# Optimization experiments

Measured on AMD Instinct MI355X. Metric: run time of the kernel, lower is better.

Reference implementation:

```python
import jax, jax.numpy as jnp
import numpy as np

N, E, F_IN, H, C, Q = 4096, 131072, 512, 64, 16, 6
ALPHA = 1.0
NITER = 2  # torch.svd_lowrank default power iterations


def setup_inputs() -> dict:
    key = jax.random.key(0)
    ks = jax.random.split(key, 12)
    rn = lambda k, s, sc=0.05: jax.random.normal(k, s, dtype=jnp.float32) * sc
    return {
        'x': jax.random.normal(ks[0], (N, F_IN), dtype=jnp.float32),
        'edge_index': jax.random.randint(ks[1], (2, E), 0, N, dtype=jnp.int32),
        'gcn1_w': rn(ks[2], (F_IN, H)), 'gcn1_b': jnp.zeros((H,), jnp.float32),
        'gcn2_w': rn(ks[3], (H, C)), 'gcn2_b': jnp.zeros((C,), jnp.float32),
        'ptd1_w1': rn(ks[4], (F_IN, H)), 'ptd1_b1': jnp.zeros((H,), jnp.float32),
        'ptd1_w2': rn(ks[5], (H, 1)), 'ptd1_b2': jnp.zeros((1,), jnp.float32),
        'ptd2_w1': rn(ks[6], (H, 32)), 'ptd2_b1': jnp.zeros((32,), jnp.float32),
        'ptd2_w2': rn(ks[7], (32, 1)), 'ptd2_b2': jnp.zeros((1,), jnp.float32),
        'omega1': jax.random.normal(ks[8], (N, Q), dtype=jnp.float32),
        'omega2': jax.random.normal(ks[9], (N, Q), dtype=jnp.float32),
    }


def _mlp2(x, w1, b1, w2, b2):
    return jax.nn.relu(x @ w1 + b1) @ w2 + b2


def _edge_gate(x, src, dst, w1, b1, w2, b2):
    # agg = ptd(x_src - x_dst)**2 ; test branch: s = alpha*sigmoid(agg), clipped to [0,1]
    agg = _mlp2(x[src] - x[dst], w1, b1, w2, b2)
    agg = agg * agg
    s = ALPHA * jax.nn.sigmoid(agg)
    return jnp.clip(s.reshape(-1), 0.0, 1.0)


def _gcn_conv(x, src, dst, ew, w, b):
    # PyG GCNConv with edge_weight: add self-loops (weight 1), symmetric norm, aggregate src->dst
    h = x @ w
    si = jnp.arange(N)
    s_full = jnp.concatenate([src, si])
    d_full = jnp.concatenate([dst, si])
    ew_full = jnp.concatenate([ew, jnp.ones((N,), ew.dtype)])
    deg = jax.ops.segment_sum(ew_full, d_full, num_segments=N)
    dis = jnp.where(deg > 0, jax.lax.rsqrt(jnp.maximum(deg, 1e-12)), 0.0)
    norm = dis[s_full] * ew_full * dis[d_full]
    out = jax.ops.segment_sum(norm[:, None] * h[s_full], d_full, num_segments=N)
    return out + b


def _svd_lowrank_V(A, omega):
    # torch.svd_lowrank(A, q=6, niter=2): randomized range finder + small SVD; returns V [N, Q]
    Qb, _ = jnp.linalg.qr(A @ omega)
    for _ in range(NITER):
        Z, _ = jnp.linalg.qr(A.T @ Qb)
        Qb, _ = jnp.linalg.qr(A @ Z)
    B = Qb.T @ A  # [Q, N]
    _, _, Vh = jnp.linalg.svd(B, full_matrices=False)
    return Vh.T  # [N, Q]


def _nuc_loss(aa, V, deflate_matmul):
    loss = jnp.float32(0.0)
    for k in range(Q):  # fixed small Q=6, structurally sequential deflation
        vi = aa @ V[:, k:k + 1]  # [N,1]
        vi = vi / jnp.linalg.norm(vi)
        vmv = (vi.T @ (aa @ vi))[0, 0]
        vv = (vi.T @ vi)[0, 0]
        loss = loss + jnp.sqrt(jnp.abs(vmv / vv))
        if k > 1:
            outer = vi @ vi.T
            aa = aa - (aa @ outer if deflate_matmul else aa * outer)
    return loss


def reference(x, edge_index, gcn1_w, gcn1_b, gcn2_w, gcn2_b,
              ptd1_w1, ptd1_b1, ptd1_w2, ptd1_b2,
              ptd2_w1, ptd2_b1, ptd2_w2, ptd2_b2, omega1, omega2):
    src, dst = edge_index[0], edge_index[1]

    s_1 = _edge_gate(x, src, dst, ptd1_w1, ptd1_b1, ptd1_w2, ptd1_b2)  # [E]
    x1 = jax.nn.relu(_gcn_conv(x, src, dst, s_1, gcn1_w, gcn1_b))  # [N,H], dropout off (eval)

    s_2 = _edge_gate(x1, src, dst, ptd2_w1, ptd2_b1, ptd2_w2, ptd2_b2)  # [E]
    x_out = _gcn_conv(x1, src, dst, s_2, gcn2_w, gcn2_b)  # [N,C]

    # consistency loss: MSE of centered gates against zeros
    consist = jnp.mean((s_1 - jnp.mean(s_1)) ** 2) + jnp.mean((s_2 - jnp.mean(s_2)) ** 2)

    # dense adjacencies (duplicate edges sum, as in to_dense_adj)
    s1d = jnp.zeros((N, N), jnp.float32).at[src, dst].add(s_1) + 1e-6
    s2d = jnp.zeros((N, N), jnp.float32).at[src, dst].add(s_2) + 1e-6
    aa1 = s1d @ s1d.T
    aa2 = s2d @ s2d.T

    V1 = _svd_lowrank_V(s1d, omega1)
    V2 = _svd_lowrank_V(s2d, omega2)
    nuc = _nuc_loss(aa1, V1, deflate_matmul=False) + _nuc_loss(aa2, V2, deflate_matmul=True)

    top2 = jax.lax.top_k(x_out, 2)[0]
    calib = -top2[:, 0] + top2[:, 1]

    return (jax.nn.log_softmax(x_out, axis=1),
            jax.nn.softmax(x_out, axis=1),
            0.01 * consist + 0.01 * nuc,
            s_1, s_2, jnp.mean(calib))
```

## Files before the change

### kernel.cpp

```cpp
#include <hip/hip_runtime.h>
#include <cmath>

constexpr int N = 4096;
constexpr int EDG = 131072;
constexpr float GEPS = 1e-6f;

__device__ __forceinline__ float* blk_sums(float* vals, int cnt) {
  __shared__ float part[4][16];
  __shared__ float tot[16];
  const int lane = threadIdx.x & 63, wv = threadIdx.x >> 6;
  for (int c = 0; c < cnt; ++c) {
    float v = vals[c];
    for (int off = 32; off; off >>= 1) v += __shfl_down(v, off);
    if (lane == 0) part[wv][c] = v;
  }
  __syncthreads();
  if (threadIdx.x == 0)
    for (int c = 0; c < cnt; ++c)
      tot[c] = part[0][c] + part[1][c] + part[2][c] + part[3][c];
  __syncthreads();
  return tot;
}

__global__ void hist_edges(const int* __restrict__ ei, int* __restrict__ cnt) {
  int e = blockIdx.x * 256 + threadIdx.x;
  atomicAdd(&cnt[ei[e]], 1);
  atomicAdd(&cnt[N + ei[EDG + e]], 1);
}

__global__ __launch_bounds__(256) void scan2x(const int* __restrict__ cnt,
                                              int* __restrict__ rowptr,
                                              int* __restrict__ cur) {
  const int b = blockIdx.x;
  const int* c = cnt + b * N;
  int* rp = rowptr + b * (N + 1);
  int* cu = cur + b * N;
  __shared__ int part[256];
  const int t = threadIdx.x;
  int local[16], s = 0;
  const int base = t * 16;
  for (int i = 0; i < 16; ++i) { local[i] = s; s += c[base + i]; }
  part[t] = s;
  __syncthreads();
  if (t == 0) {
    int acc = 0;
    for (int i = 0; i < 256; ++i) { int v = part[i]; part[i] = acc; acc += v; }
  }
  __syncthreads();
  const int off = part[t];
  for (int i = 0; i < 16; ++i) { rp[base + i] = off + local[i]; cu[base + i] = off + local[i]; }
  if (t == 255) rp[N] = off + s;
}

__global__ void scatter_edges(const int* __restrict__ ei, int* __restrict__ cur,
                              int* __restrict__ col_s, int* __restrict__ perm_s,
                              int* __restrict__ col_d, int* __restrict__ perm_d) {
  int e = blockIdx.x * 256 + threadIdx.x;
  int s = ei[e], d = ei[EDG + e];
  int ps = atomicAdd(&cur[s], 1);
  col_s[ps] = d; perm_s[ps] = e;
  int pd = atomicAdd(&cur[N + d], 1);
  col_d[pd] = s; perm_d[pd] = e;
}

__global__ void gather_w2(const float* __restrict__ s, const int* __restrict__ perm_s,
                          const int* __restrict__ perm_d, float* __restrict__ ws_,
                          float* __restrict__ wd_) {
  int p = blockIdx.x * 256 + threadIdx.x;
  ws_[p] = s[perm_s[p]];
  wd_[p] = s[perm_d[p]];
}

template<int F, int DIS>
__global__ __launch_bounds__(256) void spmm(const int* __restrict__ rowptr,
                                            const int* __restrict__ col,
                                            const float* __restrict__ w,
                                            const float* __restrict__ X,
                                            const float* __restrict__ dis,
                                            float* __restrict__ OUT,
                                            float* __restrict__ SC, int cs_idx,
                                            float eps, int osum, int ossq) {
  constexpr int ES = 64 / F;
  const int lane = threadIdx.x & 63;
  const int wv = threadIdx.x >> 6;
  const int f = lane & (F - 1);
  const int es = lane / F;
  const int r = blockIdx.x * 4 + wv;
  const int e0 = rowptr[r], e1 = rowptr[r + 1];
  float acc = 0.f;
  for (int e = e0 + es; e < e1; e += ES) {
    int c = col[e];
    float wx = w[e];
    if (DIS) wx *= dis[c];
    acc += wx * X[(size_t)c * F + f];
  }
#pragma unroll
  for (int off = F; off < 64; off <<= 1) acc += __shfl_xor(acc, off);
  float o = acc + ((cs_idx >= 0) ? eps * SC[cs_idx + f] : 0.f);
  if (es == 0) OUT[(size_t)r * F + f] = o;
  if (osum >= 0 || ossq >= 0) {
    __shared__ float bs[8], bq[8];
    if (threadIdx.x < F) { bs[threadIdx.x] = 0.f; bq[threadIdx.x] = 0.f; }
    __syncthreads();
    if (es == 0) {
      if (osum >= 0) atomicAdd(&bs[f], o);
      if (ossq >= 0) atomicAdd(&bq[f], o * o);
    }
    __syncthreads();
    if (threadIdx.x < F) {
      if (osum >= 0) atomicAdd(&SC[osum + threadIdx.x], bs[threadIdx.x]);
      if (ossq >= 0) atomicAdd(&SC[ossq + threadIdx.x], bq[threadIdx.x]);
    }
  }
}

template<int FA, int FB>
__global__ __launch_bounds__(256) void spmm2(const int* __restrict__ rowptr,
                                             const int* __restrict__ col,
                                             const float* __restrict__ wA,
                                             const float* __restrict__ wB,
                                             const float* __restrict__ XA,
                                             const float* __restrict__ XB,
                                             float* __restrict__ OA,
                                             float* __restrict__ OB,
                                             float* __restrict__ SC,
                                             int csA, int csB, float eps,
                                             int osumA, int ossqA, int osumB, int ossqB) {
  const int lane = threadIdx.x & 63;
  const int wv = threadIdx.x >> 6;
  const int half = lane >> 5;
  const int la = lane & 31;
  const int F = half ? FB : FA;
  const int f = la & (F - 1);
  const int es = la / F;
  const int ES = 32 / F;
  const int r = blockIdx.x * 4 + wv;
  const int e0 = rowptr[r], e1 = rowptr[r + 1];
  const float* w = half ? wB : wA;
  const float* X = half ? XB : XA;
  float acc = 0.f;
  for (int e = e0 + es; e < e1; e += ES)
    acc += w[e] * X[(size_t)col[e] * F + f];
  for (int off = F; off < 32; off <<= 1) acc += __shfl_xor(acc, off);
  const int cs = half ? csB : csA;
  float o = acc + ((cs >= 0) ? eps * SC[cs + f] : 0.f);
  if (es == 0) {
    float* O = half ? OB : OA;
    O[(size_t)r * F + f] = o;
  }
  if (osumA >= 0 || ossqA >= 0 || osumB >= 0 || ossqB >= 0) {
    __shared__ float bs[2][8], bq[2][8];
    if (threadIdx.x < 16) { bs[threadIdx.x >> 3][threadIdx.x & 7] = 0.f;
                            bq[threadIdx.x >> 3][threadIdx.x & 7] = 0.f; }
    __syncthreads();
    const int osum = half ? osumB : osumA, ossq = half ? ossqB : ossqA;
    if (es == 0) {
      if (osum >= 0) atomicAdd(&bs[half][f], o);
      if (ossq >= 0) atomicAdd(&bq[half][f], o * o);
    }
    __syncthreads();
    if (threadIdx.x < 16) {
      int h = threadIdx.x >> 3, ff = threadIdx.x & 7;
      int os_ = h ? osumB : osumA, oq_ = h ? ossqB : ossqA;
      int Fh = h ? FB : FA;
      if (os_ >= 0 && ff < Fh) atomicAdd(&SC[os_ + ff], bs[h][ff]);
      if (oq_ >= 0 && ff < Fh) atomicAdd(&SC[oq_ + ff], bq[h][ff]);
    }
  }
}

__global__ __launch_bounds__(256) void gemm512(const float* __restrict__ A,
                                               const float* __restrict__ W1,
                                               const float* __restrict__ W2,
                                               float* __restrict__ O1,
                                               float* __restrict__ O2) {
  __shared__ float As[16][33];
  __shared__ float Ws[32][128];
  const int t = threadIdx.x;
  const int r = t >> 4;
  const int cg = t & 15;
  const int r0 = blockIdx.x * 16;
  float acc[8];
#pragma unroll
  for (int j = 0; j < 8; ++j) acc[j] = 0.f;
  for (int k0 = 0; k0 < 512; k0 += 32) {
    __syncthreads();
    {
      int idx = t;
#pragma unroll
      for (int i = 0; i < 2; ++i, idx += 256) {
        int rr = idx >> 5, kk = idx & 31;
        As[rr][kk] = A[(size_t)(r0 + rr) * 512 + k0 + kk];
      }
    }
    for (int idx = t; idx < 32 * 128; idx += 256) {
      int kk = idx >> 7, c = idx & 127;
      Ws[kk][c] = (c < 64) ? W1[(size_t)(k0 + kk) * 64 + c]
                           : W2[(size_t)(k0 + kk) * 64 + c - 64];
    }
    __syncthreads();
#pragma unroll 4
    for (int kk = 0; kk < 32; ++kk) {
      float a = As[r][kk];
      const float* wr = &Ws[kk][cg * 8];
#pragma unroll
      for (int j = 0; j < 8; ++j) acc[j] += a * wr[j];
    }
  }
  int n = r0 + r;
  if (cg < 8) {
#pragma unroll
    for (int j = 0; j < 8; ++j) O1[(size_t)n * 64 + cg * 8 + j] = acc[j];
  } else {
#pragma unroll
    for (int j = 0; j < 8; ++j) O2[(size_t)n * 64 + (cg - 8) * 8 + j] = acc[j];
  }
}

__global__ __launch_bounds__(256) void gemm64(const float* __restrict__ A,
                                              const float* __restrict__ W1,
                                              const float* __restrict__ W2,
                                              float* __restrict__ O1,
                                              float* __restrict__ O2) {
  __shared__ float As[32][65];
  __shared__ float Ws[64][48];
  const int t = threadIdx.x;
  const int r = t >> 3;
  const int cg = t & 7;
  const int r0 = blockIdx.x * 32;
  for (int idx = t; idx < 32 * 64; idx += 256)
    As[idx >> 6][idx & 63] = A[(size_t)(r0 + (idx >> 6)) * 64 + (idx & 63)];
  for (int idx = t; idx < 64 * 48; idx += 256) {
    int kk = idx / 48, c = idx % 48;
    Ws[kk][c] = (c < 32) ? W1[kk * 32 + c] : W2[kk * 16 + c - 32];
  }
  __syncthreads();
  float acc[6] = {0.f, 0.f, 0.f, 0.f, 0.f, 0.f};
  for (int k = 0; k < 64; ++k) {
    float a = As[r][k];
#pragma unroll
    for (int j = 0; j < 6; ++j) acc[j] += a * Ws[k][cg + 8 * j];
  }
  int n = r0 + r;
#pragma unroll
  for (int j = 0; j < 6; ++j) {
    int c = cg + 8 * j;
    if (c < 32) O1[(size_t)n * 32 + c] = acc[j];
    else O2[(size_t)n * 16 + c - 32] = acc[j];
  }
}

__global__ void edge_gate1(const float* __restrict__ xw, const int* __restrict__ ei,
                           const float* __restrict__ b1, const float* __restrict__ w2,
                           const float* __restrict__ b2, float* __restrict__ s_out,
                           float* __restrict__ deg, float* __restrict__ SCs) {
  const int lane = threadIdx.x & 63;
  const int wave = threadIdx.x >> 6;
  const float b1v = b1[lane];
  const float w2v = w2[lane];
  const float b2s = b2[0];
  float lsum = 0.f, lssq = 0.f;
  for (int it = 0; it < 16; ++it) {
    const int e = blockIdx.x * 64 + it * 4 + wave;
    const int s = ei[e];
    const int d = ei[EDG + e];
    float g = xw[(size_t)s * 64 + lane] - xw[(size_t)d * 64 + lane] + b1v;
    g = fmaxf(g, 0.f) * w2v;
#pragma unroll
    for (int off = 32; off; off >>= 1) g += __shfl_down(g, off);
    if (lane == 0) {
      float agg = g + b2s;
      agg *= agg;
      float sv = 1.f / (1.f + __expf(-agg));
      s_out[e] = sv;
      atomicAdd(&deg[d], sv);
      lsum += sv; lssq += sv * sv;
    }
  }
  __shared__ float red[8];
  if (lane == 0) { red[wave] = lsum; red[4 + wave] = lssq; }
  __syncthreads();
  if (threadIdx.x == 0) {
    atomicAdd(&SCs[0], red[0] + red[1] + red[2] + red[3]);
    atomicAdd(&SCs[1], red[4] + red[5] + red[6] + red[7]);
  }
}

__global__ void edge_gate2(const float* __restrict__ xw, const int* __restrict__ ei,
                           const float* __restrict__ b1, const float* __restrict__ w2,
                           const float* __restrict__ b2, float* __restrict__ s_out,
                           float* __restrict__ deg, float* __restrict__ SCs) {
  const int half = threadIdx.x & 31;
  const int wi = threadIdx.x >> 5;
  const float b1v = b1[half];
  const float w2v = w2[half];
  const float b2s = b2[0];
  float lsum = 0.f, lssq = 0.f;
  for (int it = 0; it < 16; ++it) {
    const int e = blockIdx.x * 128 + it * 8 + wi;
    const int s = ei[e];
    const int d = ei[EDG + e];
    float g = xw[(size_t)s * 32 + half] - xw[(size_t)d * 32 + half] + b1v;
    g = fmaxf(g, 0.f) * w2v;
#pragma unroll
    for (int off = 16; off; off >>= 1) g += __shfl_down(g, off, 32);
    if (half == 0) {
      float agg = g + b2s;
      agg *= agg;
      float sv = 1.f / (1.f + __expf(-agg));
      s_out[e] = sv;
      atomicAdd(&deg[d], sv);
      lsum += sv; lssq += sv * sv;
    }
  }
  __shared__ float red[16];
  if (half == 0) { red[wi] = lsum; red[8 + wi] = lssq; }
  __syncthreads();
  if (threadIdx.x == 0) {
    float a = 0.f, b = 0.f;
    for (int i = 0; i < 8; ++i) { a += red[i]; b += red[8 + i]; }
    atomicAdd(&SCs[0], a);
    atomicAdd(&SCs[1], b);
  }
}

__global__ void make_dis(const float* __restrict__ deg, float* __restrict__ dis) {
  int n = blockIdx.x * 256 + threadIdx.x;
  dis[n] = rsqrtf(deg[n] + 1.0f);
}

__global__ void conv_epi64(const float* __restrict__ P, const float* __restrict__ h,
                           const float* __restrict__ dis, const float* __restrict__ bias,
                           float* __restrict__ out) {
  int i = blockIdx.x * 256 + threadIdx.x;
  int n = i >> 6, f = i & 63;
  float d = dis[n];
  float v = d * (P[i] + d * h[i]) + bias[f];
  out[i] = fmaxf(v, 0.f);
}

__global__ void conv2_softmax(const float* __restrict__ P, const float* __restrict__ h,
                              const float* __restrict__ dis, const float* __restrict__ bias,
                              float* __restrict__ ls, float* __restrict__ sm,
                              float* __restrict__ SC) {
  const int t = threadIdx.x;
  const int r = blockIdx.x * 256 + t;
  const float d = dis[r];
  float v[16];
  float mx = -3.0e38f, mx2 = -3.0e38f;
#pragma unroll
  for (int c = 0; c < 16; ++c) {
    v[c] = d * (P[(size_t)r * 16 + c] + d * h[(size_t)r * 16 + c]) + bias[c];
    if (v[c] > mx) { mx2 = mx; mx = v[c]; }
    else if (v[c] > mx2) mx2 = v[c];
  }
  float se = 0.f;
#pragma unroll
  for (int c = 0; c < 16; ++c) se += expf(v[c] - mx);
  const float lse = mx + logf(se);
#pragma unroll
  for (int c = 0; c < 16; ++c) {
    float z = v[c] - lse;
    ls[(size_t)r * 16 + c] = z;
    sm[(size_t)r * 16 + c] = expf(z);
  }
  float calib = mx2 - mx;
  float* tot = blk_sums(&calib, 1);
  if (t == 0) atomicAdd(&SC[4], tot[0]);
}

__global__ void gram2(const float* __restrict__ YA, const float* __restrict__ YB,
                      double* __restrict__ GA, double* __restrict__ GB) {
  const int t = threadIdx.x;
  const int lane = t & 63, wv = t >> 6;
  const int n = blockIdx.x * 256 + t;
  float g[42];
  {
    float ya[6], yb[6];
#pragma unroll
    for (int j = 0; j < 6; ++j) { ya[j] = YA[(size_t)n * 8 + j]; yb[j] = YB[(size_t)n * 8 + j]; }
    int p = 0;
#pragma unroll
    for (int i = 0; i < 6; ++i)
#pragma unroll
      for (int j = i; j < 6; ++j) { g[p] = ya[i] * ya[j]; g[21 + p] = yb[i] * yb[j]; ++p; }
  }
#pragma unroll
  for (int p = 0; p < 42; ++p)
    for (int off = 32; off; off >>= 1) g[p] += __shfl_down(g[p], off);
  __shared__ float part[4][42];
  if (lane == 0)
    for (int p = 0; p < 42; ++p) part[wv][p] = g[p];
  __syncthreads();
  if (t < 42) {
    float s = part[0][t] + part[1][t] + part[2][t] + part[3][t];
    if (t < 21) atomicAdd(&GA[t], (double)s);
    else atomicAdd(&GB[t - 21], (double)s);
  }
}

__global__ void chol2(float* __restrict__ YA, const double* __restrict__ GA, int csA,
                      float* __restrict__ YB, const double* __restrict__ GB, int csB,
                      float* __restrict__ SC) {
  __shared__ float Rs[2][36];
  if (threadIdx.x < 2) {
    const double* G = threadIdx.x ? GB : GA;
    double Gf[6][6];
    int p = 0;
    for (int i = 0; i < 6; ++i)
      for (int j = i; j < 6; ++j) { Gf[i][j] = G[p]; Gf[j][i] = G[p]; ++p; }
    double Rm[6][6];
    for (int i = 0; i < 6; ++i) for (int j = 0; j < 6; ++j) Rm[i][j] = 0.0;
    for (int j = 0; j < 6; ++j) {
      double s = Gf[j][j];
      for (int k = 0; k < j; ++k) s -= Rm[k][j] * Rm[k][j];
      double dj = sqrt(fmax(s, 1e-30));
      Rm[j][j] = dj;
      for (int i = j + 1; i < 6; ++i) {
        double v = Gf[j][i];
        for (int k = 0; k < j; ++k) v -= Rm[k][j] * Rm[k][i];
        Rm[j][i] = v / dj;
      }
    }
    for (int i = 0; i < 6; ++i)
      for (int j = 0; j < 6; ++j) Rs[threadIdx.x][i * 6 + j] = (float)Rm[i][j];
  }
  __syncthreads();
  int n = blockIdx.x * 256 + threadIdx.x;
  float vals[12];
  {
    float y[6], q[6];
#pragma unroll
    for (int j = 0; j < 6; ++j) y[j] = YA[(size_t)n * 8 + j];
#pragma unroll
    for (int j = 0; j < 6; ++j) {
      float s = y[j];
#pragma unroll
      for (int i = 0; i < 6; ++i)
        if (i < j) s -= q[i] * Rs[0][i * 6 + j];
      q[j] = s / Rs[0][j * 6 + j];
    }
#pragma unroll
    for (int j = 0; j < 6; ++j) { YA[(size_t)n * 8 + j] = q[j]; vals[j] = q[j]; }
  }
  {
    float y[6], q[6];
#pragma unroll
    for (int j = 0; j < 6; ++j) y[j] = YB[(size_t)n * 8 + j];
#pragma unroll
    for (int j = 0; j < 6; ++j) {
      float s = y[j];
#pragma unroll
      for (int i = 0; i < 6; ++i)
        if (i < j) s -= q[i] * Rs[1][i * 6 + j];
      q[j] = s / Rs[1][j * 6 + j];
    }
#pragma unroll
    for (int j = 0; j < 6; ++j) { YB[(size_t)n * 8 + j] = q[j]; vals[6 + j] = q[j]; }
  }
  float* tot = blk_sums(vals, 12);
  if (threadIdx.x == 0)
    for (int j = 0; j < 6; ++j) {
      atomicAdd(&SC[csA + j], tot[j]);
      atomicAdd(&SC[csB + j], tot[6 + j]);
    }
}

__global__ __launch_bounds__(128) void jacobi2(const double* __restrict__ GA,
                                               const double* __restrict__ GB,
                                               float* __restrict__ SMFA,
                                               float* __restrict__ SMFB) {
  const int wv = threadIdx.x >> 6;
  const int lane = threadIdx.x & 63;
  const double* G = wv ? GB : GA;
  float* SMF = wv ? SMFB : SMFA;
  double a[6], v[6];
#pragma unroll
  for (int j = 0; j < 6; ++j) { a[j] = 0.0; v[j] = 0.0; }
  if (lane < 6) {
    const int r = lane;
    for (int j = 0; j < 6; ++j) {
      int i0 = r < j ? r : j, j0 = r < j ? j : r;
      a[j] = G[i0 * 6 - i0 * (i0 - 1) / 2 + (j0 - i0)];
    }
    v[r] = 1.0;
  }
  for (int sweep = 0; sweep < 10; ++sweep) {
#pragma unroll
    for (int p = 0; p < 5; ++p)
#pragma unroll
      for (int q = p + 1; q < 6; ++q) {
        double apq = __shfl(a[q], p, 64);
        double app = __shfl(a[p], p, 64);
        double aqq = __shfl(a[q], q, 64);
        double c = 1.0, s = 0.0;
        if (fabs(apq) > 1e-300) {
          double tau = (aqq - app) / (2.0 * apq);
          double tt = (tau >= 0.0) ? 1.0 / (tau + sqrt(1.0 + tau * tau))
                                   : 1.0 / (tau - sqrt(1.0 + tau * tau));
          c = 1.0 / sqrt(1.0 + tt * tt); s = tt * c;
        }
        double ap_ = a[p], aq_ = a[q];
        a[p] = c * ap_ - s * aq_;
        a[q] = s * ap_ + c * aq_;
#pragma unroll
        for (int i = 0; i < 6; ++i) {
          double rp = __shfl(a[i], p, 64);
          double rq = __shfl(a[i], q, 64);
          if (lane == p) a[i] = c * rp - s * rq;
          if (lane == q) a[i] = s * rp + c * rq;
        }
        double vp_ = v[p], vq_ = v[q];
        v[p] = c * vp_ - s * vq_;
        v[q] = s * vp_ + c * vq_;
      }
  }
  __shared__ double diag[2][6];
  __shared__ double Vs[2][6][6];
  if (lane < 6) {
    diag[wv][lane] = a[lane];
    for (int j = 0; j < 6; ++j) Vs[wv][lane][j] = v[j];
  }
  __syncthreads();
  if (lane == 0) {
    int idx[6] = {0, 1, 2, 3, 4, 5};
    for (int x = 0; x < 5; ++x)
      for (int b = 0; b < 5 - x; ++b)
        if (diag[wv][idx[b]] < diag[wv][idx[b + 1]]) {
          int tmp = idx[b]; idx[b] = idx[b + 1]; idx[b + 1] = tmp;
        }
    for (int k = 0; k < 6; ++k) {
      double lam = diag[wv][idx[k]];
      SMF[36 + k] = (float)(1.0 / sqrt(fmax(lam, 1e-30)));
      for (int j = 0; j < 6; ++j) SMF[j * 6 + k] = (float)Vs[wv][j][idx[k]];
    }
  }
}

__global__ void v_scale2(const float* __restrict__ BtA, const float* __restrict__ SMFA,
                         const float* __restrict__ BtB, const float* __restrict__ SMFB,
                         float* __restrict__ V8A, float* __restrict__ V8B) {
  __shared__ float WsA[36], rsA[6], WsB[36], rsB[6];
  if (threadIdx.x < 36) { WsA[threadIdx.x] = SMFA[threadIdx.x]; WsB[threadIdx.x] = SMFB[threadIdx.x]; }
  if (threadIdx.x < 6) { rsA[threadIdx.x] = SMFA[36 + threadIdx.x]; rsB[threadIdx.x] = SMFB[36 + threadIdx.x]; }
  __syncthreads();
  int n = blockIdx.x * 256 + threadIdx.x;
  float ba[6], bb[6];
#pragma unroll
  for (int j = 0; j < 6; ++j) { ba[j] = BtA[(size_t)n * 8 + j]; bb[j] = BtB[(size_t)n * 8 + j]; }
#pragma unroll
  for (int k = 0; k < 6; ++k) {
    float sa = 0.f, sb = 0.f;
#pragma unroll
    for (int j = 0; j < 6; ++j) { sa += ba[j] * WsA[j * 6 + k]; sb += bb[j] * WsB[j * 6 + k]; }
    V8A[(size_t)n * 8 + k] = sa * rsA[k];
    V8B[(size_t)n * 8 + k] = sb * rsB[k];
  }
  V8A[(size_t)n * 8 + 6] = 0.f; V8A[(size_t)n * 8 + 7] = 0.f;
  V8B[(size_t)n * 8 + 6] = 0.f; V8B[(size_t)n * 8 + 7] = 0.f;
}

__global__ void pad8c2(const float* __restrict__ o1, float* __restrict__ d1,
                       const float* __restrict__ o2, float* __restrict__ d2,
                       float* __restrict__ SC, int s1, int s2) {
  int n = blockIdx.x * 256 + threadIdx.x;
  float vals[12];
#pragma unroll
  for (int k = 0; k < 6; ++k) {
    vals[k] = o1[(size_t)n * 6 + k];     d1[(size_t)n * 8 + k] = vals[k];
    vals[6 + k] = o2[(size_t)n * 6 + k]; d2[(size_t)n * 8 + k] = vals[6 + k];
  }
  d1[(size_t)n * 8 + 6] = 0.f; d1[(size_t)n * 8 + 7] = 0.f;
  d2[(size_t)n * 8 + 6] = 0.f; d2[(size_t)n * 8 + 7] = 0.f;
  float* tot = blk_sums(vals, 12);
  if (threadIdx.x == 0)
    for (int c = 0; c < 6; ++c) {
      atomicAdd(&SC[s1 + c], tot[c]);
      atomicAdd(&SC[s2 + c], tot[6 + c]);
    }
}

__global__ void pack3c2(const float* __restrict__ V8A, float* __restrict__ WA,
                        const float* __restrict__ V8B, float* __restrict__ WB,
                        float* __restrict__ SC, int sA, int sB) {
  int n = blockIdx.x * 256 + threadIdx.x;
  float vals[6];
#pragma unroll
  for (int k = 0; k < 3; ++k) {
    vals[k] = V8A[(size_t)n * 8 + k];     WA[(size_t)n * 4 + k] = vals[k];
    vals[3 + k] = V8B[(size_t)n * 8 + k]; WB[(size_t)n * 4 + k] = vals[3 + k];
  }
  WA[(size_t)n * 4 + 3] = 0.f;
  WB[(size_t)n * 4 + 3] = 0.f;
  float* tot = blk_sums(vals, 6);
  if (threadIdx.x == 0)
    for (int c = 0; c < 3; ++c) {
      atomicAdd(&SC[sA + c], tot[c]);
      atomicAdd(&SC[sB + c], tot[3 + c]);
    }
}

__global__ void build_Wc(float* __restrict__ out, int FCpad, int nterms, int nu,
                         const float* __restrict__ base, int bstride, int boff,
                         const float* __restrict__ U, const float* __restrict__ SCin,
                         int rs_idx, float* __restrict__ SC, int sum_idx) {
  int n = blockIdx.x * 256 + threadIdx.x;
  float bv = base[(size_t)n * bstride + boff];
  if (rs_idx >= 0) bv *= rsqrtf(SCin[rs_idx]);
  float uv[3];
  for (int b = 0; b < 3; ++b) uv[b] = (b < nu) ? U[(size_t)b * N + n] : 0.f;
  float vals[8];
  for (int t = 0; t < FCpad; ++t) {
    float v = 0.f;
    if (t < nterms) {
      v = bv;
      for (int b = 0; b < nu; ++b)
        if ((t >> b) & 1) v *= uv[b];
    }
    out[(size_t)n * FCpad + t] = v;
    vals[t] = v;
  }
  float* tot = blk_sums(vals, nterms);
  if (threadIdx.x == 0)
    for (int c = 0; c < nterms; ++c) atomicAdd(&SC[sum_idx + c], tot[c]);
}

__global__ void buildAB(float* __restrict__ WA, int FCpad, int nt, int nu,
                        const float* __restrict__ V8A, int kcol,
                        const float* __restrict__ UvA, float* __restrict__ SC, int sWa,
                        float* __restrict__ WB, const float* __restrict__ V8B,
                        const float* __restrict__ UvB, int nd, int sWb, int Cidx) {
  const int bid = blockIdx.x;
  const int n = (bid & 15) * 256 + threadIdx.x;
  if (bid < 16) {
    float bv = V8A[(size_t)n * 8 + kcol];
    float uv[3];
    for (int b = 0; b < 3; ++b) uv[b] = (b < nu) ? UvA[(size_t)b * N + n] : 0.f;
    float vals[8];
    for (int t = 0; t < FCpad; ++t) {
      float v = 0.f;
      if (t < nt) {
        v = bv;
        for (int b = 0; b < nu; ++b)
          if ((t >> b) & 1) v *= uv[b];
      }
      WA[(size_t)n * FCpad + t] = v;
      vals[t] = v;
    }
    float* tot = blk_sums(vals, nt);
    if (threadIdx.x == 0)
      for (int c = 0; c < nt; ++c) atomicAdd(&SC[sWa + c], tot[c]);
  } else {
    float v = V8B[(size_t)n * 8 + kcol];
    WB[(size_t)n * 4 + 0] = v;
    WB[(size_t)n * 4 + 1] = 0.f;
    WB[(size_t)n * 4 + 2] = 0.f;
    WB[(size_t)n * 4 + 3] = 0.f;
    float vals[4];
    vals[0] = v;
    for (int t = 0; t < 3; ++t) vals[1 + t] = (t < nd) ? UvB[(size_t)t * N + n] * v : 0.f;
    float* tot = blk_sums(vals, 1 + nd);
    if (threadIdx.x == 0) {
      atomicAdd(&SC[sWb], tot[0]);
      for (int t = 0; t < nd; ++t) atomicAdd(&SC[Cidx + t], tot[1 + t]);
    }
  }
}

__global__ void epiAB(const float* __restrict__ YA, int FA, int nt, int nu,
                      const float* __restrict__ UvA, float* __restrict__ yvA, int nyA2,
                      const float* __restrict__ YB, const float* __restrict__ Pv,
                      const float* __restrict__ UvB, int nd, float* __restrict__ yvB,
                      int Cidx, int nyB2, int dp, float* __restrict__ SC) {
  const int bid = blockIdx.x;
  const int n = (bid & 15) * 256 + threadIdx.x;
  if (bid < 16) {
    float uv[3];
    for (int b = 0; b < 3; ++b) uv[b] = (b < nu) ? UvA[(size_t)b * N + n] : 0.f;
    float s = 0.f;
    for (int t = 0; t < nt; ++t) {
      float w = YA[(size_t)n * FA + t];
      int pc = 0;
      for (int b = 0; b < nu; ++b)
        if ((t >> b) & 1) { w *= uv[b]; ++pc; }
      s += (pc & 1) ? -w : w;
    }
    yvA[n] = s;
    float v = s * s;
    float* tot = blk_sums(&v, 1);
    if (threadIdx.x == 0) atomicAdd(&SC[nyA2], tot[0]);
  } else {
    float y = YB[(size_t)n * 4];
    for (int t = 0; t < nd; ++t) y -= SC[Cidx + t] * Pv[(size_t)t * N + n];
    yvB[n] = y;
    float vals[7];
    vals[0] = y * y;
    for (int t = 0; t < 3; ++t) {
      vals[1 + 2 * t] = (t < nd) ? y * Pv[(size_t)t * N + n] : 0.f;
      vals[2 + 2 * t] = (t < nd) ? UvB[(size_t)t * N + n] * y : 0.f;
    }
    float* tot = blk_sums(vals, 1 + 2 * nd);
    if (threadIdx.x == 0) {
      atomicAdd(&SC[nyB2], tot[0]);
      for (int i = 0; i < 2 * nd; ++i) atomicAdd(&SC[dp + i], tot[1 + i]);
    }
  }
}

__global__ void buildAB2(float* __restrict__ WA, int FCpad, int nt, int nu,
                         const float* __restrict__ yvA, const float* __restrict__ UvA,
                         int sW2a, float* __restrict__ WB,
                         const float* __restrict__ yvB, int sW2b,
                         float* __restrict__ SC) {
  const int bid = blockIdx.x;
  const int n = (bid & 15) * 256 + threadIdx.x;
  if (bid < 16) {
    float bv = yvA[n];
    float uv[3];
    for (int b = 0; b < 3; ++b) uv[b] = (b < nu) ? UvA[(size_t)b * N + n] : 0.f;
    float vals[8];
    for (int t = 0; t < FCpad; ++t) {
      float v = 0.f;
      if (t < nt) {
        v = bv;
        for (int b = 0; b < nu; ++b)
          if ((t >> b) & 1) v *= uv[b];
      }
      WA[(size_t)n * FCpad + t] = v;
      vals[t] = v;
    }
    float* tot = blk_sums(vals, nt);
    if (threadIdx.x == 0)
      for (int c = 0; c < nt; ++c) atomicAdd(&SC[sW2a + c], tot[c]);
  } else {
    float v = yvB[n];
    WB[(size_t)n * 4 + 0] = v;
    WB[(size_t)n * 4 + 1] = 0.f;
    WB[(size_t)n * 4 + 2] = 0.f;
    WB[(size_t)n * 4 + 3] = 0.f;
    float vv = v;
    float* tot = blk_sums(&vv, 1);
    if (threadIdx.x == 0) atomicAdd(&SC[sW2b], tot[0]);
  }
}

__global__ void vscale2(float* __restrict__ o1, const float* __restrict__ i1,
                        int s1, int f1, int r1,
                        float* __restrict__ o2, const float* __restrict__ i2,
                        int s2, int f2, int r2, const float* __restrict__ SC) {
  int n = blockIdx.x * 256 + threadIdx.x;
  float v1 = i1[(size_t)n * s1 + f1];
  if (r1 >= 0) v1 *= rsqrtf(SC[r1]);
  o1[n] = v1;
  float v2 = i2[(size_t)n * s2 + f2];
  if (r2 >= 0) v2 *= rsqrtf(SC[r2]);
  o2[n] = v2;
}

__global__ void vscale1(float* __restrict__ out, const float* __restrict__ in,
                        int stride, int off, const float* __restrict__ SC, int rs_idx) {
  int n = blockIdx.x * 256 + threadIdx.x;
  float v = in[(size_t)n * stride + off];
  if (rs_idx >= 0) v *= rsqrtf(SC[rs_idx]);
  out[n] = v;
}

__global__ void axpy_sq(float* __restrict__ out, const float* __restrict__ Y, int stride,
                        int off, const float* __restrict__ q0, const float* __restrict__ q1,
                        const float* __restrict__ q2, float* __restrict__ SC,
                        int c0, int c1, int c2, int np, int coef_rs, int out_rs,
                        int ssq_idx) {
  int n = blockIdx.x * 256 + threadIdx.x;
  float crs = (coef_rs >= 0) ? rsqrtf(SC[coef_rs]) : 1.f;
  float s = Y[(size_t)n * stride + off];
  if (np > 0) s -= SC[c0] * crs * q0[n];
  if (np > 1) s -= SC[c1] * crs * q1[n];
  if (np > 2) s -= SC[c2] * crs * q2[n];
  if (out_rs >= 0) s *= rsqrtf(SC[out_rs]);
  out[n] = s;
  if (ssq_idx >= 0) {
    float v = s * s;
    float* tot = blk_sums(&v, 1);
    if (threadIdx.x == 0) atomicAdd(&SC[ssq_idx], tot[0]);
  }
}

__global__ void accum2b(float* __restrict__ SC, int zA, int nyA, int zB, int nyB) {
  if (threadIdx.x || blockIdx.x) return;
  float add = 0.f;
  for (int k = 0; k < 3; ++k) add += sqrtf(fabsf(SC[zA + k] / SC[nyA + k]));
  for (int k = 0; k < 3; ++k) add += sqrtf(fabsf(SC[zB + k] / SC[nyB + k]));
  SC[5] += add;
}

__global__ void accum2k(float* __restrict__ SC, int zzA, int nt, int nyA,
                        int zzB, int nyB, int dp, int nd) {
  if (threadIdx.x || blockIdx.x) return;
  float vmv = 0.f;
  for (int t = 0; t < nt; ++t) {
    int pc = __popc(t);
    vmv += (pc & 1) ? -SC[zzA + t] : SC[zzA + t];
  }
  float add = sqrtf(fabsf(vmv / SC[nyA]));
  float vb = SC[zzB];
  for (int t = 0; t < nd; ++t) vb -= SC[dp + 2 * t] * SC[dp + 2 * t + 1];
  add += sqrtf(fabsf(vb / SC[nyB]));
  SC[5] += add;
}

__global__ void finalize_k(const float* __restrict__ SC, float* __restrict__ out) {
  if (threadIdx.x || blockIdx.x) return;
  const float Ef = (float)EDG;
  float m1 = SC[0] / Ef, v1 = SC[1] / Ef - m1 * m1;
  float m2 = SC[2] / Ef, v2 = SC[3] / Ef - m2 * m2;
  out[131072] = 0.01f * (v1 + v2) + 0.01f * SC[5];
  out[393217] = SC[4] / (float)N;
}

extern "C" void kernel_launch(void* const* d_in, const int* in_sizes, int n_in,
                              void* d_out, int out_size, void* d_ws, size_t ws_size,
                              hipStream_t stream) {
  const float* x      = (const float*)d_in[0];
  const int*   ei     = (const int*)  d_in[1];
  const float* gcn1_w = (const float*)d_in[2];
  const float* gcn1_b = (const float*)d_in[3];
  const float* gcn2_w = (const float*)d_in[4];
  const float* gcn2_b = (const float*)d_in[5];
  const float* p1w1   = (const float*)d_in[6];
  const float* p1b1   = (const float*)d_in[7];
  const float* p1w2   = (const float*)d_in[8];
  const float* p1b2   = (const float*)d_in[9];
  const float* p2w1   = (const float*)d_in[10];
  const float* p2b1   = (const float*)d_in[11];
  const float* p2w2   = (const float*)d_in[12];
  const float* p2b2   = (const float*)d_in[13];
  const float* omega1 = (const float*)d_in[14];
  const float* omega2 = (const float*)d_in[15];
  float* out = (float*)d_out;

  float* ws = (float*)d_ws;
  size_t o = 0;
  auto alloc = [&](size_t nf) { float* p = ws + o; o += nf; return p; };
  float* xw1  = alloc((size_t)N * 64);
  float* h1   = alloc((size_t)N * 64);
  float* x1   = alloc((size_t)N * 64);
  float* P    = alloc((size_t)N * 64);
  float* x1w  = alloc((size_t)N * 32);
  float* h2   = alloc((size_t)N * 16);
  float* P2   = alloc((size_t)N * 16);
  float* dis1 = alloc(N);
  float* dis2 = alloc(N);
  float* OmA  = alloc((size_t)N * 8);
  float* OmB  = alloc((size_t)N * 8);
  float* QA   = alloc((size_t)N * 8);
  float* QB   = alloc((size_t)N * 8);
  float* ZA   = alloc((size_t)N * 8);
  float* ZB   = alloc((size_t)N * 8);
  float* BtA  = alloc((size_t)N * 8);
  float* BtB  = alloc((size_t)N * 8);
  float* V8A  = alloc((size_t)N * 8);
  float* V8B  = alloc((size_t)N * 8);
  float* WA   = alloc((size_t)N * 8);
  float* WB   = alloc((size_t)N * 4);
  float* TA   = alloc((size_t)N * 8);
  float* TB   = alloc((size_t)N * 4);
  float* YA   = alloc((size_t)N * 8);
  float* YB   = alloc((size_t)N * 4);
  float* ZZA  = alloc((size_t)N * 8);
  float* ZZB  = alloc((size_t)N * 4);
  float* P4   = alloc((size_t)N * 4);
  float* yvA  = alloc(N);
  float* yvB  = alloc(N);
  float* UvA  = alloc((size_t)3 * N);
  float* UvB  = alloc((size_t)3 * N);
  float* Pv   = alloc((size_t)3 * N);
  float* SMFA = alloc(64);
  float* SMFB = alloc(64);
  int* rowptr = (int*)alloc(2 * (N + 1) + 2);
  int* cur    = (int*)alloc(2 * N);
  int* col_s  = (int*)alloc(EDG);
  int* perm_s = (int*)alloc(EDG);
  int* col_d  = (int*)alloc(EDG);
  int* perm_d = (int*)alloc(EDG);
  float* w1s  = alloc(EDG);
  float* w1d  = alloc(EDG);
  float* w2s  = alloc(EDG);
  float* w2d  = alloc(EDG);
  o = (o + 1) & ~(size_t)1;
  float* zb = ws + o;
  double* Gd = (double*)zb;            o += 288 * 2;
  int* cnt   = (int*)(ws + o);         o += 2 * N;
  float* deg1 = alloc(N);
  float* deg2 = alloc(N);
  float* SC   = alloc(1024);
  const size_t zero_bytes = (576 + 2 * N + 2 * N + 1024) * sizeof(float);
  if (ws_size < o * sizeof(float)) return;

  const int* rp_s = rowptr;
  const int* rp_d = rowptr + (N + 1);

  int cs = 8;
  auto NS = [&]() { int s = cs; cs += 8; return s; };
  int gslot = 0;
  auto NG = [&]() { int g = gslot; gslot += 24; return g; };

  hipMemsetAsync(zb, 0, zero_bytes, stream);
  hist_edges<<<512, 256, 0, stream>>>(ei, cnt);
  scan2x<<<2, 256, 0, stream>>>(cnt, rowptr, cur);
  scatter_edges<<<512, 256, 0, stream>>>(ei, cur, col_s, perm_s, col_d, perm_d);

  gemm512<<<256, 256, 0, stream>>>(x, p1w1, gcn1_w, xw1, h1);
  edge_gate1<<<2048, 256, 0, stream>>>(xw1, ei, p1b1, p1w2, p1b2,
                                       out + 131073, deg1, SC + 0);
  gather_w2<<<512, 256, 0, stream>>>(out + 131073, perm_s, perm_d, w1s, w1d);
  make_dis<<<16, 256, 0, stream>>>(deg1, dis1);
  spmm<64, 1><<<1024, 256, 0, stream>>>(rp_d, col_d, w1d, h1, dis1, P, SC, -1, 0.f, -1, -1);
  conv_epi64<<<1024, 256, 0, stream>>>(P, h1, dis1, gcn1_b, x1);

  gemm64<<<128, 256, 0, stream>>>(x1, p2w1, gcn2_w, x1w, h2);
  edge_gate2<<<1024, 256, 0, stream>>>(x1w, ei, p2b1, p2w2, p2b2,
                                       out + 262145, deg2, SC + 2);
  gather_w2<<<512, 256, 0, stream>>>(out + 262145, perm_s, perm_d, w2s, w2d);
  make_dis<<<16, 256, 0, stream>>>(deg2, dis2);
  spmm<16, 1><<<1024, 256, 0, stream>>>(rp_d, col_d, w2d, h2, dis2, P2, SC, -1, 0.f, -1, -1);
  conv2_softmax<<<16, 256, 0, stream>>>(P2, h2, dis2, gcn2_b, out, out + 65536, SC);

  {
    int s0a = NS(), s0b = NS();
    pad8c2<<<16, 256, 0, stream>>>(omega1, OmA, omega2, OmB, SC, s0a, s0b);
    spmm2<8, 8><<<1024, 256, 0, stream>>>(rp_s, col_s, w1s, w2s, OmA, OmB, QA, QB,
                                          SC, s0a, s0b, GEPS, -1, -1, -1, -1);
    int g0a = NG(), g0b = NG();
    gram2<<<16, 256, 0, stream>>>(QA, QB, Gd + g0a, Gd + g0b);
    int cqa = NS(), cqb = NS();
    chol2<<<16, 256, 0, stream>>>(QA, Gd + g0a, cqa, QB, Gd + g0b, cqb, SC);
    for (int itp = 0; itp < 2; ++itp) {
      spmm2<8, 8><<<1024, 256, 0, stream>>>(rp_d, col_d, w1d, w2d, QA, QB, ZA, ZB,
                                            SC, cqa, cqb, GEPS, -1, -1, -1, -1);
      int gza = NG(), gzb = NG();
      gram2<<<16, 256, 0, stream>>>(ZA, ZB, Gd + gza, Gd + gzb);
      int cza = NS(), czb = NS();
      chol2<<<16, 256, 0, stream>>>(ZA, Gd + gza, cza, ZB, Gd + gzb, czb, SC);
      spmm2<8, 8><<<1024, 256, 0, stream>>>(rp_s, col_s, w1s, w2s, ZA, ZB, QA, QB,
                                            SC, cza, czb, GEPS, -1, -1, -1, -1);
      int gqa = NG(), gqb = NG();
      gram2<<<16, 256, 0, stream>>>(QA, QB, Gd + gqa, Gd + gqb);
      cqa = NS(); cqb = NS();
      chol2<<<16, 256, 0, stream>>>(QA, Gd + gqa, cqa, QB, Gd + gqb, cqb, SC);
    }
    spmm2<8, 8><<<1024, 256, 0, stream>>>(rp_d, col_d, w1d, w2d, QA, QB, BtA, BtB,
                                          SC, cqa, cqb, GEPS, -1, -1, -1, -1);
    int gba = NG(), gbb = NG();
    gram2<<<16, 256, 0, stream>>>(BtA, BtB, Gd + gba, Gd + gbb);
    jacobi2<<<1, 128, 0, stream>>>(Gd + gba, Gd + gbb, SMFA, SMFB);
    v_scale2<<<16, 256, 0, stream>>>(BtA, SMFA, BtB, SMFB, V8A, V8B);
  }

  int nyB0;
  {
    int sWa = NS(), sWb = NS();
    pack3c2<<<16, 256, 0, stream>>>(V8A, WA, V8B, WB, SC, sWa, sWb);
    int sTa = NS(), sTb = NS();
    spmm2<4, 4><<<1024, 256, 0, stream>>>(rp_d, col_d, w1d, w2d, WA, WB, TA, TB,
                                          SC, sWa, sWb, GEPS, sTa, -1, sTb, -1);
    int sYa = NS(), sYb = NS(), nyA = NS(), nyB = NS();
    spmm2<4, 4><<<1024, 256, 0, stream>>>(rp_s, col_s, w1s, w2s, TA, TB, YA, YB,
                                          SC, sTa, sTb, GEPS, sYa, nyA, sYb, nyB);
    int zzA = NS(), zzB = NS();
    spmm2<4, 4><<<1024, 256, 0, stream>>>(rp_d, col_d, w1d, w2d, YA, YB, ZZA, ZZB,
                                          SC, sYa, sYb, GEPS, -1, zzA, -1, zzB);
    accum2b<<<1, 1, 0, stream>>>(SC, zzA, nyA, zzB, nyB);
    vscale2<<<16, 256, 0, stream>>>(UvA, YA, 4, 2, nyA + 2,
                                    UvB, YB, 4, 2, nyB + 2, SC);
    nyB0 = nyB;
  }

  {
    int sWp = NS();
    build_Wc<<<16, 256, 0, stream>>>(WB, 4, 1, 0, ZZB, 4, 2, nullptr, SC, nyB0 + 2, SC, sWp);
    spmm<4, 0><<<1024, 256, 0, stream>>>(rp_s, col_s, w2s, WB, nullptr, P4, SC, sWp, GEPS, -1, -1);
    vscale1<<<16, 256, 0, stream>>>(Pv, P4, 4, 0, SC, -1);
  }

  for (int k = 3; k <= 5; ++k) {
    const int nu = k - 2, nt = 1 << nu, nd = k - 2;
    const int FA = (k < 5) ? 4 : 8;
    int sWa = NS(), sWb = NS(), C = NS(), sTa = NS(), sTb = NS();
    int nyA2 = NS(), nyB2 = NS(), sW2a = NS(), sW2b = NS(), zzA2 = NS(), zzB2 = NS(), dp = NS();
    buildAB<<<32, 256, 0, stream>>>(WA, FA, nt, nu, V8A, k, UvA, SC, sWa,
                                    WB, V8B, UvB, nd, sWb, C);
    if (FA == 4) {
      spmm2<4, 4><<<1024, 256, 0, stream>>>(rp_d, col_d, w1d, w2d, WA, WB, TA, TB,
                                            SC, sWa, sWb, GEPS, sTa, -1, sTb, -1);
      spmm2<4, 4><<<1024, 256, 0, stream>>>(rp_s, col_s, w1s, w2s, TA, TB, YA, YB,
                                            SC, sTa, sTb, GEPS, -1, -1, -1, -1);
    } else {
      spmm2<8, 4><<<1024, 256, 0, stream>>>(rp_d, col_d, w1d, w2d, WA, WB, TA, TB,
                                            SC, sWa, sWb, GEPS, sTa, -1, sTb, -1);
      spmm2<8, 4><<<1024, 256, 0, stream>>>(rp_s, col_s, w1s, w2s, TA, TB, YA, YB,
                                            SC, sTa, sTb, GEPS, -1, -1, -1, -1);
    }
    epiAB<<<32, 256, 0, stream>>>(YA, FA, nt, nu, UvA, yvA, nyA2,
                                  YB, Pv, UvB, nd, yvB, C, nyB2, dp, SC);
    buildAB2<<<32, 256, 0, stream>>>(WA, FA, nt, nu, yvA, UvA, sW2a,
                                     WB, yvB, sW2b, SC);
    if (FA == 4)
      spmm2<4, 4><<<1024, 256, 0, stream>>>(rp_d, col_d, w1d, w2d, WA, WB, ZZA, ZZB,
                                            SC, sW2a, sW2b, GEPS, -1, zzA2, -1, zzB2);
    else
      spmm2<8, 4><<<1024, 256, 0, stream>>>(rp_d, col_d, w1d, w2d, WA, WB, ZZA, ZZB,
                                            SC, sW2a, sW2b, GEPS, -1, zzA2, -1, zzB2);
    accum2k<<<1, 1, 0, stream>>>(SC, zzA2, nt, nyA2, zzB2, nyB2, dp, nd);
    if (k < 5) {
      vscale2<<<16, 256, 0, stream>>>(UvA + (size_t)(k - 2) * N, yvA, 1, 0, nyA2,
                                      UvB + (size_t)(k - 2) * N, yvB, 1, 0, nyB2, SC);
      int sW3 = NS();
      build_Wc<<<16, 256, 0, stream>>>(WB, 4, 1, 0, ZZB, 4, 0, nullptr, SC, nyB2, SC, sW3);
      spmm<4, 0><<<1024, 256, 0, stream>>>(rp_s, col_s, w2s, WB, nullptr, P4, SC, sW3, GEPS, -1, -1);
      axpy_sq<<<16, 256, 0, stream>>>(Pv + (size_t)(k - 2) * N, P4, 4, 0,
                                      Pv, Pv + N, Pv + 2 * N,
                                      SC, dp + 1, dp + 3, dp + 5, nd, nyB2, -1, -1);
    }
  }

  finalize_k<<<1, 1, 0, stream>>>(SC, out);
}
```

Baseline: 863.4 us.

## Restructure pipeline with fused conv, softmax, Cholesky-QR power iteration kernels

Replaces large parts of the host-side launch sequence and many kernels. The gather kernel now also computes degree rsqrt and omega column sums. GCN convolutions get dedicated fused kernels with self-loop and bias folded in, and softmax/log-softmax/top-2 calibration share one kernel. The randomized SVD range finder now uses an spmm kernel that applies an in-kernel Cholesky-QR normalization from the accumulated Gram matrix, and the 512-wide GEMM is split along K with atomic accumulation. Several small post-processing launches in the deflation loop are merged. The aim is fewer launches and fewer passes over memory, at the cost of atomics, double-precision Gram accumulation, and more complex numerics that could differ from the reference.

```diff
diff --git a/kernel.cpp b/kernel.cpp
--- a/kernel.cpp
+++ b/kernel.cpp
@@ -63,12 +63,375 @@
   col_d[pd] = s; perm_d[pd] = e;
 }
 
-__global__ void gather_w2(const float* __restrict__ s, const int* __restrict__ perm_s,
-                          const int* __restrict__ perm_d, float* __restrict__ ws_,
-                          float* __restrict__ wd_) {
+__global__ void gatherdis_om(const float* __restrict__ s, const int* __restrict__ perm_s,
+                             const int* __restrict__ perm_d, float* __restrict__ ws_,
+                             float* __restrict__ wd_, const float* __restrict__ deg,
+                             float* __restrict__ dis, const float* __restrict__ om1,
+                             const float* __restrict__ om2, float* __restrict__ SC,
+                             int omA, int omB) {
   int p = blockIdx.x * 256 + threadIdx.x;
   ws_[p] = s[perm_s[p]];
   wd_[p] = s[perm_d[p]];
+  if (p < N) dis[p] = rsqrtf(deg[p] + 1.0f);
+  if (om1 && blockIdx.x < 16) {
+    int n = p;
+    float vals[12];
+#pragma unroll
+    for (int k = 0; k < 6; ++k) {
+      vals[k] = om1[(size_t)n * 6 + k];
+      vals[6 + k] = om2[(size_t)n * 6 + k];
+    }
+    float* tot = blk_sums(vals, 12);
+    if (threadIdx.x == 0)
+      for (int c = 0; c < 6; ++c) {
+        atomicAdd(&SC[omA + c], tot[c]);
+        atomicAdd(&SC[omB + c], tot[6 + c]);
+      }
+  }
+}
+
+__global__ __launch_bounds__(256) void gemm512k(const float* __restrict__ A,
+                                                const float* __restrict__ W1,
+                                                const float* __restrict__ W2,
+                                                float* __restrict__ O1,
+                                                float* __restrict__ O2) {
+  __shared__ float As[16][33];
+  __shared__ float Ws[32][128];
+  const int t = threadIdx.x;
+  const int rt = t >> 4;
+  const int ct = t & 15;
+  const int r0 = blockIdx.x * 16;
+  const int kh = blockIdx.y * 256;
+  float acc[8];
+#pragma unroll
+  for (int j = 0; j < 8; ++j) acc[j] = 0.f;
+  for (int kc = 0; kc < 256; kc += 32) {
+    const int kb = kh + kc;
+    __syncthreads();
+    for (int i = t; i < 512; i += 256) {
+      int rr = i >> 5, kk = i & 31;
+      As[rr][kk] = A[(size_t)(r0 + rr) * 512 + kb + kk];
+    }
+    for (int i = t; i < 1024; i += 256) {
+      int row = i >> 5, c4 = i & 31;
+      float4 v;
+      if (c4 < 16) v = *(const float4*)&W1[(size_t)(kb + row) * 64 + c4 * 4];
+      else         v = *(const float4*)&W2[(size_t)(kb + row) * 64 + (c4 - 16) * 4];
+      *(float4*)&Ws[row][c4 * 4] = v;
+    }
+    __syncthreads();
+#pragma unroll
+    for (int kk = 0; kk < 32; ++kk) {
+      float a = As[rt][kk];
+      float4 b0 = *(const float4*)&Ws[kk][ct * 4];
+      float4 b1 = *(const float4*)&Ws[kk][64 + ct * 4];
+      acc[0] += a * b0.x; acc[1] += a * b0.y;
+      acc[2] += a * b0.z; acc[3] += a * b0.w;
+      acc[4] += a * b1.x; acc[5] += a * b1.y;
+      acc[6] += a * b1.z; acc[7] += a * b1.w;
+    }
+  }
+  const int r = r0 + rt;
+#pragma unroll
+  for (int j = 0; j < 4; ++j) {
+    atomicAdd(&O1[(size_t)r * 64 + ct * 4 + j], acc[j]);
+    atomicAdd(&O2[(size_t)r * 64 + ct * 4 + j], acc[4 + j]);
+  }
+}
+
+__global__ __launch_bounds__(256) void gemm64(const float* __restrict__ A,
+                                              const float* __restrict__ W1,
+                                              const float* __restrict__ W2,
+                                              float* __restrict__ O1,
+                                              float* __restrict__ O2) {
+  __shared__ float As[32][65];
+  __shared__ float Ws[64][48];
+  const int t = threadIdx.x;
+  const int r = t >> 3;
+  const int cg = t & 7;
+  const int r0 = blockIdx.x * 32;
+  for (int idx = t; idx < 32 * 64; idx += 256)
+    As[idx >> 6][idx & 63] = A[(size_t)(r0 + (idx >> 6)) * 64 + (idx & 63)];
+  for (int idx = t; idx < 64 * 48; idx += 256) {
+    int kk = idx / 48, c = idx % 48;
+    Ws[kk][c] = (c < 32) ? W1[kk * 32 + c] : W2[kk * 16 + c - 32];
+  }
+  __syncthreads();
+  float acc[6] = {0.f, 0.f, 0.f, 0.f, 0.f, 0.f};
+  for (int k = 0; k < 64; ++k) {
+    float a = As[r][k];
+#pragma unroll
+    for (int j = 0; j < 6; ++j) acc[j] += a * Ws[k][cg + 8 * j];
+  }
+  int n = r0 + r;
+#pragma unroll
+  for (int j = 0; j < 6; ++j) {
+    int c = cg + 8 * j;
+    if (c < 32) O1[(size_t)n * 32 + c] = acc[j];
+    else O2[(size_t)n * 16 + c - 32] = acc[j];
+  }
+}
+
+__global__ void edge_gate1(const float* __restrict__ xw, const int* __restrict__ ei,
+                           const float* __restrict__ b1, const float* __restrict__ w2,
+                           const float* __restrict__ b2, float* __restrict__ s_out,
+                           float* __restrict__ deg, float* __restrict__ SCs) {
+  const int lane = threadIdx.x & 63;
+  const int wave = threadIdx.x >> 6;
+  const float b1v = b1[lane];
+  const float w2v = w2[lane];
+  const float b2s = b2[0];
+  float lsum = 0.f, lssq = 0.f;
+  for (int it = 0; it < 16; ++it) {
+    const int e = blockIdx.x * 64 + it * 4 + wave;
+    const int s = ei[e];
+    const int d = ei[EDG + e];
+    float g = xw[(size_t)s * 64 + lane] - xw[(size_t)d * 64 + lane] + b1v;
+    g = fmaxf(g, 0.f) * w2v;
+#pragma unroll
+    for (int off = 32; off; off >>= 1) g += __shfl_down(g, off);
+    if (lane == 0) {
+      float agg = g + b2s;
+      agg *= agg;
+      float sv = 1.f / (1.f + __expf(-agg));
+      s_out[e] = sv;
+      atomicAdd(&deg[d], sv);
+      lsum += sv; lssq += sv * sv;
+    }
+  }
+  __shared__ float red[8];
+  if (lane == 0) { red[wave] = lsum; red[4 + wave] = lssq; }
+  __syncthreads();
+  if (threadIdx.x == 0) {
+    atomicAdd(&SCs[0], red[0] + red[1] + red[2] + red[3]);
+    atomicAdd(&SCs[1], red[4] + red[5] + red[6] + red[7]);
+  }
+}
+
+__global__ void edge_gate2(const float* __restrict__ xw, const int* __restrict__ ei,
+                           const float* __restrict__ b1, const float* __restrict__ w2,
+                           const float* __restrict__ b2, float* __restrict__ s_out,
+                           float* __restrict__ deg, float* __restrict__ SCs) {
+  const int half = threadIdx.x & 31;
+  const int wi = threadIdx.x >> 5;
+  const float b1v = b1[half];
+  const float w2v = w2[half];
+  const float b2s = b2[0];
+  float lsum = 0.f, lssq = 0.f;
+  for (int it = 0; it < 16; ++it) {
+    const int e = blockIdx.x * 128 + it * 8 + wi;
+    const int s = ei[e];
+    const int d = ei[EDG + e];
+    float g = xw[(size_t)s * 32 + half] - xw[(size_t)d * 32 + half] + b1v;
+    g = fmaxf(g, 0.f) * w2v;
+#pragma unroll
+    for (int off = 16; off; off >>= 1) g += __shfl_down(g, off, 32);
+    if (half == 0) {
+      float agg = g + b2s;
+      agg *= agg;
+      float sv = 1.f / (1.f + __expf(-agg));
+      s_out[e] = sv;
+      atomicAdd(&deg[d], sv);
+      lsum += sv; lssq += sv * sv;
+    }
+  }
+  __shared__ float red[16];
+  if (half == 0) { red[wi] = lsum; red[8 + wi] = lssq; }
+  __syncthreads();
+  if (threadIdx.x == 0) {
+    float a = 0.f, b = 0.f;
+    for (int i = 0; i < 8; ++i) { a += red[i]; b += red[8 + i]; }
+    atomicAdd(&SCs[0], a);
+    atomicAdd(&SCs[1], b);
+  }
+}
+
+__global__ void conv1f(const int* __restrict__ rp, const int* __restrict__ cl,
+                       const float* __restrict__ w, const float* __restrict__ h1,
+                       const float* __restrict__ dis, const float* __restrict__ bias,
+                       float* __restrict__ x1) {
+  const int lane = threadIdx.x & 63, wv = threadIdx.x >> 6;
+  const int r = blockIdx.x * 4 + wv;
+  const int e0 = rp[r], e1 = rp[r + 1];
+  float acc = 0.f;
+  for (int e = e0; e < e1; ++e) {
+    int c = cl[e];
+    acc += w[e] * dis[c] * h1[(size_t)c * 64 + lane];
+  }
+  float d = dis[r];
+  float v = d * (acc + d * h1[(size_t)r * 64 + lane]) + bias[lane];
+  x1[(size_t)r * 64 + lane] = fmaxf(v, 0.f);
+}
+
+__global__ void conv2f(const int* __restrict__ rp, const int* __restrict__ cl,
+                       const float* __restrict__ w, const float* __restrict__ h2,
+                       const float* __restrict__ dis, const float* __restrict__ bias,
+                       float* __restrict__ xo) {
+  const int lane = threadIdx.x & 63, wv = threadIdx.x >> 6;
+  const int f = lane & 15, es = lane >> 4;
+  const int r = blockIdx.x * 4 + wv;
+  const int e0 = rp[r], e1 = rp[r + 1];
+  float acc = 0.f;
+  for (int e = e0 + es; e < e1; e += 4) {
+    int c = cl[e];
+    acc += w[e] * dis[c] * h2[(size_t)c * 16 + f];
+  }
+  acc += __shfl_xor(acc, 16);
+  acc += __shfl_xor(acc, 32);
+  if (es == 0) {
+    float d = dis[r];
+    xo[(size_t)r * 16 + f] = d * (acc + d * h2[(size_t)r * 16 + f]) + bias[f];
+  }
+}
+
+__global__ void softmax_calib(const float* __restrict__ xo, float* __restrict__ ls,
+                              float* __restrict__ sm, float* __restrict__ SC) {
+  const int t = threadIdx.x;
+  const int r = blockIdx.x * 256 + t;
+  float v[16];
+  float mx = -3.0e38f, mx2 = -3.0e38f;
+#pragma unroll
+  for (int c = 0; c < 16; ++c) {
+    v[c] = xo[(size_t)r * 16 + c];
+    if (v[c] > mx) { mx2 = mx; mx = v[c]; }
+    else if (v[c] > mx2) mx2 = v[c];
+  }
+  float se = 0.f;
+#pragma unroll
+  for (int c = 0; c < 16; ++c) se += expf(v[c] - mx);
+  const float lse = mx + logf(se);
+#pragma unroll
+  for (int c = 0; c < 16; ++c) {
+    float z = v[c] - lse;
+    ls[(size_t)r * 16 + c] = z;
+    sm[(size_t)r * 16 + c] = expf(z);
+  }
+  float calib = mx2 - mx;
+  float* tot = blk_sums(&calib, 1);
+  if (t == 0) atomicAdd(&SC[4], tot[0]);
+}
+
+template<int NORM, int SX>
+__global__ __launch_bounds__(256) void spmm8f(
+    const int* __restrict__ rp, const int* __restrict__ cl,
+    const float* __restrict__ wA, const float* __restrict__ wB,
+    const float* __restrict__ XA, const float* __restrict__ XB,
+    float* __restrict__ OA, float* __restrict__ OB,
+    const double* __restrict__ GpA, const double* __restrict__ GpB,
+    double* __restrict__ GnA, double* __restrict__ GnB,
+    float* __restrict__ SC, int cspA, int cspB, int csoA, int csoB) {
+  __shared__ float Rinv[2][36];
+  __shared__ float csn[2][8];
+  __shared__ float bs[2][8];
+  __shared__ float gpart[8][21];
+  const int t = threadIdx.x;
+  if (NORM) {
+    if (t < 2) {
+      const double* G = t ? GpB : GpA;
+      const float* csp = SC + (t ? cspB : cspA);
+      double Gf[6][6];
+      int p = 0;
+      for (int i = 0; i < 6; ++i)
+        for (int j = i; j < 6; ++j) { Gf[i][j] = G[p]; Gf[j][i] = G[p]; ++p; }
+      double Rm[6][6];
+      for (int i = 0; i < 6; ++i) for (int j = 0; j < 6; ++j) Rm[i][j] = 0.0;
+      for (int j = 0; j < 6; ++j) {
+        double s = Gf[j][j];
+        for (int k = 0; k < j; ++k) s -= Rm[k][j] * Rm[k][j];
+        double dj = sqrt(fmax(s, 1e-30));
+        Rm[j][j] = dj;
+        for (int i = j + 1; i < 6; ++i) {
+          double v = Gf[j][i];
+          for (int k = 0; k < j; ++k) v -= Rm[k][j] * Rm[k][i];
+          Rm[j][i] = v / dj;
+        }
+      }
+      double Ri[6][6];
+      for (int j = 0; j < 6; ++j) {
+        Ri[j][j] = 1.0 / Rm[j][j];
+        for (int i = j - 1; i >= 0; --i) {
+          double s = 0.0;
+          for (int k = i + 1; k <= j; ++k) s += Rm[i][k] * Ri[k][j];
+          Ri[i][j] = -s / Rm[i][i];
+        }
+      }
+      for (int i = 0; i < 6; ++i)
+        for (int j = 0; j < 6; ++j)
+          Rinv[t][i * 6 + j] = (j >= i) ? (float)Ri[i][j] : 0.f;
+      for (int f = 0; f < 8; ++f) {
+        float s = 0.f;
+        if (f < 6)
+          for (int j = 0; j <= f; ++j) s += csp[j] * (float)Ri[j][f];
+        csn[t][f] = s;
+      }
+    }
+  } else {
+    if (t < 16) {
+      int h = t >> 3, f = t & 7;
+      csn[h][f] = (f < 6) ? SC[(h ? cspB : cspA) + f] : 0.f;
+    }
+  }
+  if (t < 16) bs[t >> 3][t & 7] = 0.f;
+  __syncthreads();
+  const int lane = t & 63, wv = t >> 6;
+  const int half = lane >> 5, la = lane & 31;
+  const int f = la & 7, es = la >> 3;
+  const float* w = half ? wB : wA;
+  const float* X = half ? XB : XA;
+  float* O = half ? OB : OA;
+  const float* Ri = Rinv[half];
+  const float epsf = csn[half][f] * GEPS;
+  float gp[6];
+#pragma unroll
+  for (int j = 0; j < 6; ++j) gp[j] = 0.f;
+  for (int rr = 0; rr < 2; ++rr) {
+    const int r = blockIdx.x * 8 + wv * 2 + rr;
+    const int e0 = rp[r], e1 = rp[r + 1];
+    float acc = 0.f;
+    if (f < 6) {
+      for (int e = e0 + es; e < e1; e += 4) {
+        int c = cl[e];
+        const float* xr = X + (size_t)c * SX;
+        float xn;
+        if (NORM) {
+          xn = 0.f;
+          for (int j = 0; j <= f; ++j) xn += xr[j] * Ri[j * 6 + f];
+        } else {
+          xn = xr[f];
+        }
+        acc += w[e] * xn;
+      }
+    }
+    acc += __shfl_xor(acc, 8);
+    acc += __shfl_xor(acc, 16);
+    float o = acc + epsf;
+    float ov[6];
+#pragma unroll
+    for (int j = 0; j < 6; ++j) ov[j] = __shfl(o, half * 32 + j);
+    if (es == 0) {
+      O[((size_t)r << 3) + f] = o;
+      if (f < 6) {
+        atomicAdd(&bs[half][f], o);
+#pragma unroll
+        for (int j = 0; j < 6; ++j)
+          if (j >= f) gp[j - f] += o * ov[j];
+      }
+    }
+  }
+  if (es == 0 && f < 6) {
+    int p0 = f * 6 - (f * (f - 1)) / 2;
+    for (int j = 0; j < 6 - f; ++j) gpart[wv * 2 + half][p0 + j] = gp[j];
+  }
+  __syncthreads();
+  if (t < 42) {
+    int h = t / 21, p = t % 21;
+    float s = gpart[h][p] + gpart[2 + h][p] + gpart[4 + h][p] + gpart[6 + h][p];
+    atomicAdd(&(h ? GnB : GnA)[p], (double)s);
+  }
+  if (t < 16) {
+    int h = t >> 3, ff = t & 7;
+    if (ff < 6) atomicAdd(&SC[(h ? csoB : csoA) + ff], bs[h][ff]);
+  }
 }
 
 template<int F, int DIS>
@@ -169,303 +532,6 @@
   }
 }
 
-__global__ __launch_bounds__(256) void gemm512(const float* __restrict__ A,
-                                               const float* __restrict__ W1,
-                                               const float* __restrict__ W2,
-                                               float* __restrict__ O1,
-                                               float* __restrict__ O2) {
-  __shared__ float As[16][33];
-  __shared__ float Ws[32][128];
-  const int t = threadIdx.x;
-  const int r = t >> 4;
-  const int cg = t & 15;
-  const int r0 = blockIdx.x * 16;
-  float acc[8];
-#pragma unroll
-  for (int j = 0; j < 8; ++j) acc[j] = 0.f;
-  for (int k0 = 0; k0 < 512; k0 += 32) {
-    __syncthreads();
-    {
-      int idx = t;
-#pragma unroll
-      for (int i = 0; i < 2; ++i, idx += 256) {
-        int rr = idx >> 5, kk = idx & 31;
-        As[rr][kk] = A[(size_t)(r0 + rr) * 512 + k0 + kk];
-      }
-    }
-    for (int idx = t; idx < 32 * 128; idx += 256) {
-      int kk = idx >> 7, c = idx & 127;
-      Ws[kk][c] = (c < 64) ? W1[(size_t)(k0 + kk) * 64 + c]
-                           : W2[(size_t)(k0 + kk) * 64 + c - 64];
-    }
-    __syncthreads();
-#pragma unroll 4
-    for (int kk = 0; kk < 32; ++kk) {
-      float a = As[r][kk];
-      const float* wr = &Ws[kk][cg * 8];
-#pragma unroll
-      for (int j = 0; j < 8; ++j) acc[j] += a * wr[j];
-    }
-  }
-  int n = r0 + r;
-  if (cg < 8) {
-#pragma unroll
-    for (int j = 0; j < 8; ++j) O1[(size_t)n * 64 + cg * 8 + j] = acc[j];
-  } else {
-#pragma unroll
-    for (int j = 0; j < 8; ++j) O2[(size_t)n * 64 + (cg - 8) * 8 + j] = acc[j];
-  }
-}
-
-__global__ __launch_bounds__(256) void gemm64(const float* __restrict__ A,
-                                              const float* __restrict__ W1,
-                                              const float* __restrict__ W2,
-                                              float* __restrict__ O1,
-                                              float* __restrict__ O2) {
-  __shared__ float As[32][65];
-  __shared__ float Ws[64][48];
-  const int t = threadIdx.x;
-  const int r = t >> 3;
-  const int cg = t & 7;
-  const int r0 = blockIdx.x * 32;
-  for (int idx = t; idx < 32 * 64; idx += 256)
-    As[idx >> 6][idx & 63] = A[(size_t)(r0 + (idx >> 6)) * 64 + (idx & 63)];
-  for (int idx = t; idx < 64 * 48; idx += 256) {
-    int kk = idx / 48, c = idx % 48;
-    Ws[kk][c] = (c < 32) ? W1[kk * 32 + c] : W2[kk * 16 + c - 32];
-  }
-  __syncthreads();
-  float acc[6] = {0.f, 0.f, 0.f, 0.f, 0.f, 0.f};
-  for (int k = 0; k < 64; ++k) {
-    float a = As[r][k];
-#pragma unroll
-    for (int j = 0; j < 6; ++j) acc[j] += a * Ws[k][cg + 8 * j];
-  }
-  int n = r0 + r;
-#pragma unroll
-  for (int j = 0; j < 6; ++j) {
-    int c = cg + 8 * j;
-    if (c < 32) O1[(size_t)n * 32 + c] = acc[j];
-    else O2[(size_t)n * 16 + c - 32] = acc[j];
-  }
-}
-
-__global__ void edge_gate1(const float* __restrict__ xw, const int* __restrict__ ei,
-                           const float* __restrict__ b1, const float* __restrict__ w2,
-                           const float* __restrict__ b2, float* __restrict__ s_out,
-                           float* __restrict__ deg, float* __restrict__ SCs) {
-  const int lane = threadIdx.x & 63;
-  const int wave = threadIdx.x >> 6;
-  const float b1v = b1[lane];
-  const float w2v = w2[lane];
-  const float b2s = b2[0];
-  float lsum = 0.f, lssq = 0.f;
-  for (int it = 0; it < 16; ++it) {
-    const int e = blockIdx.x * 64 + it * 4 + wave;
-    const int s = ei[e];
-    const int d = ei[EDG + e];
-    float g = xw[(size_t)s * 64 + lane] - xw[(size_t)d * 64 + lane] + b1v;
-    g = fmaxf(g, 0.f) * w2v;
-#pragma unroll
-    for (int off = 32; off; off >>= 1) g += __shfl_down(g, off);
-    if (lane == 0) {
-      float agg = g + b2s;
-      agg *= agg;
-      float sv = 1.f / (1.f + __expf(-agg));
-      s_out[e] = sv;
-      atomicAdd(&deg[d], sv);
-      lsum += sv; lssq += sv * sv;
-    }
-  }
-  __shared__ float red[8];
-  if (lane == 0) { red[wave] = lsum; red[4 + wave] = lssq; }
-  __syncthreads();
-  if (threadIdx.x == 0) {
-    atomicAdd(&SCs[0], red[0] + red[1] + red[2] + red[3]);
-    atomicAdd(&SCs[1], red[4] + red[5] + red[6] + red[7]);
-  }
-}
-
-__global__ void edge_gate2(const float* __restrict__ xw, const int* __restrict__ ei,
-                           const float* __restrict__ b1, const float* __restrict__ w2,
-                           const float* __restrict__ b2, float* __restrict__ s_out,
-                           float* __restrict__ deg, float* __restrict__ SCs) {
-  const int half = threadIdx.x & 31;
-  const int wi = threadIdx.x >> 5;
-  const float b1v = b1[half];
-  const float w2v = w2[half];
-  const float b2s = b2[0];
-  float lsum = 0.f, lssq = 0.f;
-  for (int it = 0; it < 16; ++it) {
-    const int e = blockIdx.x * 128 + it * 8 + wi;
-    const int s = ei[e];
-    const int d = ei[EDG + e];
-    float g = xw[(size_t)s * 32 + half] - xw[(size_t)d * 32 + half] + b1v;
-    g = fmaxf(g, 0.f) * w2v;
-#pragma unroll
-    for (int off = 16; off; off >>= 1) g += __shfl_down(g, off, 32);
-    if (half == 0) {
-      float agg = g + b2s;
-      agg *= agg;
-      float sv = 1.f / (1.f + __expf(-agg));
-      s_out[e] = sv;
-      atomicAdd(&deg[d], sv);
-      lsum += sv; lssq += sv * sv;
-    }
-  }
-  __shared__ float red[16];
-  if (half == 0) { red[wi] = lsum; red[8 + wi] = lssq; }
-  __syncthreads();
-  if (threadIdx.x == 0) {
-    float a = 0.f, b = 0.f;
-    for (int i = 0; i < 8; ++i) { a += red[i]; b += red[8 + i]; }
-    atomicAdd(&SCs[0], a);
-    atomicAdd(&SCs[1], b);
-  }
-}
-
-__global__ void make_dis(const float* __restrict__ deg, float* __restrict__ dis) {
-  int n = blockIdx.x * 256 + threadIdx.x;
-  dis[n] = rsqrtf(deg[n] + 1.0f);
-}
-
-__global__ void conv_epi64(const float* __restrict__ P, const float* __restrict__ h,
-                           const float* __restrict__ dis, const float* __restrict__ bias,
-                           float* __restrict__ out) {
-  int i = blockIdx.x * 256 + threadIdx.x;
-  int n = i >> 6, f = i & 63;
-  float d = dis[n];
-  float v = d * (P[i] + d * h[i]) + bias[f];
-  out[i] = fmaxf(v, 0.f);
-}
-
-__global__ void conv2_softmax(const float* __restrict__ P, const float* __restrict__ h,
-                              const float* __restrict__ dis, const float* __restrict__ bias,
-                              float* __restrict__ ls, float* __restrict__ sm,
-                              float* __restrict__ SC) {
-  const int t = threadIdx.x;
-  const int r = blockIdx.x * 256 + t;
-  const float d = dis[r];
-  float v[16];
-  float mx = -3.0e38f, mx2 = -3.0e38f;
-#pragma unroll
-  for (int c = 0; c < 16; ++c) {
-    v[c] = d * (P[(size_t)r * 16 + c] + d * h[(size_t)r * 16 + c]) + bias[c];
-    if (v[c] > mx) { mx2 = mx; mx = v[c]; }
-    else if (v[c] > mx2) mx2 = v[c];
-  }
-  float se = 0.f;
-#pragma unroll
-  for (int c = 0; c < 16; ++c) se += expf(v[c] - mx);
-  const float lse = mx + logf(se);
-#pragma unroll
-  for (int c = 0; c < 16; ++c) {
-    float z = v[c] - lse;
-    ls[(size_t)r * 16 + c] = z;
-    sm[(size_t)r * 16 + c] = expf(z);
-  }
-  float calib = mx2 - mx;
-  float* tot = blk_sums(&calib, 1);
-  if (t == 0) atomicAdd(&SC[4], tot[0]);
-}
-
-__global__ void gram2(const float* __restrict__ YA, const float* __restrict__ YB,
-                      double* __restrict__ GA, double* __restrict__ GB) {
-  const int t = threadIdx.x;
-  const int lane = t & 63, wv = t >> 6;
-  const int n = blockIdx.x * 256 + t;
-  float g[42];
-  {
-    float ya[6], yb[6];
-#pragma unroll
-    for (int j = 0; j < 6; ++j) { ya[j] = YA[(size_t)n * 8 + j]; yb[j] = YB[(size_t)n * 8 + j]; }
-    int p = 0;
-#pragma unroll
-    for (int i = 0; i < 6; ++i)
-#pragma unroll
-      for (int j = i; j < 6; ++j) { g[p] = ya[i] * ya[j]; g[21 + p] = yb[i] * yb[j]; ++p; }
-  }
-#pragma unroll
-  for (int p = 0; p < 42; ++p)
-    for (int off = 32; off; off >>= 1) g[p] += __shfl_down(g[p], off);
-  __shared__ float part[4][42];
-  if (lane == 0)
-    for (int p = 0; p < 42; ++p) part[wv][p] = g[p];
-  __syncthreads();
-  if (t < 42) {
-    float s = part[0][t] + part[1][t] + part[2][t] + part[3][t];
-    if (t < 21) atomicAdd(&GA[t], (double)s);
-    else atomicAdd(&GB[t - 21], (double)s);
-  }
-}
-
-__global__ void chol2(float* __restrict__ YA, const double* __restrict__ GA, int csA,
-                      float* __restrict__ YB, const double* __restrict__ GB, int csB,
-                      float* __restrict__ SC) {
-  __shared__ float Rs[2][36];
-  if (threadIdx.x < 2) {
-    const double* G = threadIdx.x ? GB : GA;
-    double Gf[6][6];
-    int p = 0;
-    for (int i = 0; i < 6; ++i)
-      for (int j = i; j < 6; ++j) { Gf[i][j] = G[p]; Gf[j][i] = G[p]; ++p; }
-    double Rm[6][6];
-    for (int i = 0; i < 6; ++i) for (int j = 0; j < 6; ++j) Rm[i][j] = 0.0;
-    for (int j = 0; j < 6; ++j) {
-      double s = Gf[j][j];
-      for (int k = 0; k < j; ++k) s -= Rm[k][j] * Rm[k][j];
-      double dj = sqrt(fmax(s, 1e-30));
-      Rm[j][j] = dj;
-      for (int i = j + 1; i < 6; ++i) {
-        double v = Gf[j][i];
-        for (int k = 0; k < j; ++k) v -= Rm[k][j] * Rm[k][i];
-        Rm[j][i] = v / dj;
-      }
-    }
-    for (int i = 0; i < 6; ++i)
-      for (int j = 0; j < 6; ++j) Rs[threadIdx.x][i * 6 + j] = (float)Rm[i][j];
-  }
-  __syncthreads();
-  int n = blockIdx.x * 256 + threadIdx.x;
-  float vals[12];
-  {
-    float y[6], q[6];
-#pragma unroll
-    for (int j = 0; j < 6; ++j) y[j] = YA[(size_t)n * 8 + j];
-#pragma unroll
-    for (int j = 0; j < 6; ++j) {
-      float s = y[j];
-#pragma unroll
-      for (int i = 0; i < 6; ++i)
-        if (i < j) s -= q[i] * Rs[0][i * 6 + j];
-      q[j] = s / Rs[0][j * 6 + j];
-    }
-#pragma unroll
-    for (int j = 0; j < 6; ++j) { YA[(size_t)n * 8 + j] = q[j]; vals[j] = q[j]; }
-  }
-  {
-    float y[6], q[6];
-#pragma unroll
-    for (int j = 0; j < 6; ++j) y[j] = YB[(size_t)n * 8 + j];
-#pragma unroll
-    for (int j = 0; j < 6; ++j) {
-      float s = y[j];
-#pragma unroll
-      for (int i = 0; i < 6; ++i)
-        if (i < j) s -= q[i] * Rs[1][i * 6 + j];
-      q[j] = s / Rs[1][j * 6 + j];
-    }
-#pragma unroll
-    for (int j = 0; j < 6; ++j) { YB[(size_t)n * 8 + j] = q[j]; vals[6 + j] = q[j]; }
-  }
-  float* tot = blk_sums(vals, 12);
-  if (threadIdx.x == 0)
-    for (int j = 0; j < 6; ++j) {
-      atomicAdd(&SC[csA + j], tot[j]);
-      atomicAdd(&SC[csB + j], tot[6 + j]);
-    }
-}
-
 __global__ __launch_bounds__(128) void jacobi2(const double* __restrict__ GA,
                                                const double* __restrict__ GB,
                                                float* __restrict__ SMFA,
@@ -560,26 +626,6 @@
   V8B[(size_t)n * 8 + 6] = 0.f; V8B[(size_t)n * 8 + 7] = 0.f;
 }
 
-__global__ void pad8c2(const float* __restrict__ o1, float* __restrict__ d1,
-                       const float* __restrict__ o2, float* __restrict__ d2,
-                       float* __restrict__ SC, int s1, int s2) {
-  int n = blockIdx.x * 256 + threadIdx.x;
-  float vals[12];
-#pragma unroll
-  for (int k = 0; k < 6; ++k) {
-    vals[k] = o1[(size_t)n * 6 + k];     d1[(size_t)n * 8 + k] = vals[k];
-    vals[6 + k] = o2[(size_t)n * 6 + k]; d2[(size_t)n * 8 + k] = vals[6 + k];
-  }
-  d1[(size_t)n * 8 + 6] = 0.f; d1[(size_t)n * 8 + 7] = 0.f;
-  d2[(size_t)n * 8 + 6] = 0.f; d2[(size_t)n * 8 + 7] = 0.f;
-  float* tot = blk_sums(vals, 12);
-  if (threadIdx.x == 0)
-    for (int c = 0; c < 6; ++c) {
-      atomicAdd(&SC[s1 + c], tot[c]);
-      atomicAdd(&SC[s2 + c], tot[6 + c]);
-    }
-}
-
 __global__ void pack3c2(const float* __restrict__ V8A, float* __restrict__ WA,
                         const float* __restrict__ V8B, float* __restrict__ WB,
                         float* __restrict__ SC, int sA, int sB) {
@@ -600,36 +646,35 @@
     }
 }
 
-__global__ void build_Wc(float* __restrict__ out, int FCpad, int nterms, int nu,
-                         const float* __restrict__ base, int bstride, int boff,
-                         const float* __restrict__ U, const float* __restrict__ SCin,
-                         int rs_idx, float* __restrict__ SC, int sum_idx) {
+__global__ void b3post(const float* __restrict__ YA, const float* __restrict__ YB,
+                       const float* __restrict__ ZZB, float* __restrict__ UvA,
+                       float* __restrict__ UvB, float* __restrict__ WB,
+                       float* __restrict__ SC, int zzA, int nyA, int zzB, int nyB,
+                       int sWp) {
+  if (blockIdx.x == 0 && threadIdx.x == 0) {
+    float add = 0.f;
+    for (int k = 0; k < 3; ++k) add += sqrtf(fabsf(SC[zzA + k] / SC[nyA + k]));
+    for (int k = 0; k < 3; ++k) add += sqrtf(fabsf(SC[zzB + k] / SC[nyB + k]));
+    SC[5] += add;
+  }
   int n = blockIdx.x * 256 + threadIdx.x;
-  float bv = base[(size_t)n * bstride + boff];
-  if (rs_idx >= 0) bv *= rsqrtf(SCin[rs_idx]);
-  float uv[3];
-  for (int b = 0; b < 3; ++b) uv[b] = (b < nu) ? U[(size_t)b * N + n] : 0.f;
-  float vals[8];
-  for (int t = 0; t < FCpad; ++t) {
-    float v = 0.f;
-    if (t < nterms) {
-      v = bv;
-      for (int b = 0; b < nu; ++b)
-        if ((t >> b) & 1) v *= uv[b];
-    }
-    out[(size_t)n * FCpad + t] = v;
-    vals[t] = v;
-  }
-  float* tot = blk_sums(vals, nterms);
-  if (threadIdx.x == 0)
-    for (int c = 0; c < nterms; ++c) atomicAdd(&SC[sum_idx + c], tot[c]);
+  UvA[n] = YA[(size_t)n * 4 + 2] * rsqrtf(SC[nyA + 2]);
+  UvB[n] = YB[(size_t)n * 4 + 2] * rsqrtf(SC[nyB + 2]);
+  float v = ZZB[(size_t)n * 4 + 2] * rsqrtf(SC[nyB + 2]);
+  WB[(size_t)n * 4 + 0] = v;
+  WB[(size_t)n * 4 + 1] = 0.f;
+  WB[(size_t)n * 4 + 2] = 0.f;
+  WB[(size_t)n * 4 + 3] = 0.f;
+  float* tot = blk_sums(&v, 1);
+  if (threadIdx.x == 0) atomicAdd(&SC[sWp], tot[0]);
 }
 
 __global__ void buildAB(float* __restrict__ WA, int FCpad, int nt, int nu,
                         const float* __restrict__ V8A, int kcol,
                         const float* __restrict__ UvA, float* __restrict__ SC, int sWa,
                         float* __restrict__ WB, const float* __restrict__ V8B,
-                        const float* __restrict__ UvB, int nd, int sWb, int Cidx) {
+                        const float* __restrict__ UvB, int nd, int sWb, int Cidx,
+                        const float* __restrict__ P4, float* __restrict__ Pv, int copyP) {
   const int bid = blockIdx.x;
   const int n = (bid & 15) * 256 + threadIdx.x;
   if (bid < 16) {
@@ -651,6 +696,7 @@
     if (threadIdx.x == 0)
       for (int c = 0; c < nt; ++c) atomicAdd(&SC[sWa + c], tot[c]);
   } else {
+    if (copyP) Pv[n] = P4[(size_t)n * 4];
     float v = V8B[(size_t)n * 8 + kcol];
     WB[(size_t)n * 4 + 0] = v;
     WB[(size_t)n * 4 + 1] = 0.f;
@@ -738,31 +784,41 @@
     WB[(size_t)n * 4 + 1] = 0.f;
     WB[(size_t)n * 4 + 2] = 0.f;
     WB[(size_t)n * 4 + 3] = 0.f;
-    float vv = v;
-    float* tot = blk_sums(&vv, 1);
+    float* tot = blk_sums(&v, 1);
     if (threadIdx.x == 0) atomicAdd(&SC[sW2b], tot[0]);
   }
 }
 
-__global__ void vscale2(float* __restrict__ o1, const float* __restrict__ i1,
-                        int s1, int f1, int r1,
-                        float* __restrict__ o2, const float* __restrict__ i2,
-                        int s2, int f2, int r2, const float* __restrict__ SC) {
-  int n = blockIdx.x * 256 + threadIdx.x;
-  float v1 = i1[(size_t)n * s1 + f1];
-  if (r1 >= 0) v1 *= rsqrtf(SC[r1]);
-  o1[n] = v1;
-  float v2 = i2[(size_t)n * s2 + f2];
-  if (r2 >= 0) v2 *= rsqrtf(SC[r2]);
-  o2[n] = v2;
-}
-
-__global__ void vscale1(float* __restrict__ out, const float* __restrict__ in,
-                        int stride, int off, const float* __restrict__ SC, int rs_idx) {
-  int n = blockIdx.x * 256 + threadIdx.x;
-  float v = in[(size_t)n * stride + off];
-  if (rs_idx >= 0) v *= rsqrtf(SC[rs_idx]);
-  out[n] = v;
+__global__ void defpost(float* __restrict__ SC, int zzA2, int nt, int nyA2,
+                        int zzB2, int nyB2, int dp, int nd,
+                        const float* __restrict__ yvA, const float* __restrict__ yvB,
+                        float* __restrict__ UvA, float* __restrict__ UvB, int k,
+                        const float* __restrict__ ZZB, float* __restrict__ WB,
+                        int sW3, int dobuild) {
+  if (blockIdx.x == 0 && threadIdx.x == 0) {
+    float vmv = 0.f;
+    for (int t = 0; t < nt; ++t) {
+      int pc = __popc(t);
+      vmv += (pc & 1) ? -SC[zzA2 + t] : SC[zzA2 + t];
+    }
+    float add = sqrtf(fabsf(vmv / SC[nyA2]));
+    float vb = SC[zzB2];
+    for (int t = 0; t < nd; ++t) vb -= SC[dp + 2 * t] * SC[dp + 2 * t + 1];
+    add += sqrtf(fabsf(vb / SC[nyB2]));
+    SC[5] += add;
+  }
+  if (dobuild) {
+    int n = blockIdx.x * 256 + threadIdx.x;
+    UvA[(size_t)(k - 2) * N + n] = yvA[n] * rsqrtf(SC[nyA2]);
+    UvB[(size_t)(k - 2) * N + n] = yvB[n] * rsqrtf(SC[nyB2]);
+    float v = ZZB[(size_t)n * 4 + 0] * rsqrtf(SC[nyB2]);
+    WB[(size_t)n * 4 + 0] = v;
+    WB[(size_t)n * 4 + 1] = 0.f;
+    WB[(size_t)n * 4 + 2] = 0.f;
+    WB[(size_t)n * 4 + 3] = 0.f;
+    float* tot = blk_sums(&v, 1);
+    if (threadIdx.x == 0) atomicAdd(&SC[sW3], tot[0]);
+  }
 }
 
 __global__ void axpy_sq(float* __restrict__ out, const float* __restrict__ Y, int stride,
@@ -783,29 +839,6 @@
     float* tot = blk_sums(&v, 1);
     if (threadIdx.x == 0) atomicAdd(&SC[ssq_idx], tot[0]);
   }
-}
-
-__global__ void accum2b(float* __restrict__ SC, int zA, int nyA, int zB, int nyB) {
-  if (threadIdx.x || blockIdx.x) return;
-  float add = 0.f;
-  for (int k = 0; k < 3; ++k) add += sqrtf(fabsf(SC[zA + k] / SC[nyA + k]));
-  for (int k = 0; k < 3; ++k) add += sqrtf(fabsf(SC[zB + k] / SC[nyB + k]));
-  SC[5] += add;
-}
-
-__global__ void accum2k(float* __restrict__ SC, int zzA, int nt, int nyA,
-                        int zzB, int nyB, int dp, int nd) {
-  if (threadIdx.x || blockIdx.x) return;
-  float vmv = 0.f;
-  for (int t = 0; t < nt; ++t) {
-    int pc = __popc(t);
-    vmv += (pc & 1) ? -SC[zzA + t] : SC[zzA + t];
-  }
-  float add = sqrtf(fabsf(vmv / SC[nyA]));
-  float vb = SC[zzB];
-  for (int t = 0; t < nd; ++t) vb -= SC[dp + 2 * t] * SC[dp + 2 * t + 1];
-  add += sqrtf(fabsf(vb / SC[nyB]));
-  SC[5] += add;
 }
 
 __global__ void finalize_k(const float* __restrict__ SC, float* __restrict__ out) {
@@ -843,15 +876,18 @@
   auto alloc = [&](size_t nf) { float* p = ws + o; o += nf; return p; };
   float* xw1  = alloc((size_t)N * 64);
   float* h1   = alloc((size_t)N * 64);
+  double* Gd  = (double*)(ws + o); o += 576;
+  int* cnt    = (int*)(ws + o);    o += 2 * N;
+  float* deg1 = alloc(N);
+  float* deg2 = alloc(N);
+  float* SC   = alloc(1024);
+  const size_t zero_bytes = o * sizeof(float);
   float* x1   = alloc((size_t)N * 64);
-  float* P    = alloc((size_t)N * 64);
   float* x1w  = alloc((size_t)N * 32);
   float* h2   = alloc((size_t)N * 16);
-  float* P2   = alloc((size_t)N * 16);
+  float* xo   = alloc((size_t)N * 16);
   float* dis1 = alloc(N);
   float* dis2 = alloc(N);
-  float* OmA  = alloc((size_t)N * 8);
-  float* OmB  = alloc((size_t)N * 8);
   float* QA   = alloc((size_t)N * 8);
   float* QB   = alloc((size_t)N * 8);
   float* ZA   = alloc((size_t)N * 8);
@@ -886,14 +922,6 @@
   float* w1d  = alloc(EDG);
   float* w2s  = alloc(EDG);
   float* w2d  = alloc(EDG);
-  o = (o + 1) & ~(size_t)1;
-  float* zb = ws + o;
-  double* Gd = (double*)zb;            o += 288 * 2;
-  int* cnt   = (int*)(ws + o);         o += 2 * N;
-  float* deg1 = alloc(N);
-  float* deg2 = alloc(N);
-  float* SC   = alloc(1024);
-  const size_t zero_bytes = (576 + 2 * N + 2 * N + 1024) * sizeof(float);
   if (ws_size < o * sizeof(float)) return;
 
   const int* rp_s = rowptr;
@@ -904,122 +932,109 @@
   int gslot = 0;
   auto NG = [&]() { int g = gslot; gslot += 24; return g; };
 
-  hipMemsetAsync(zb, 0, zero_bytes, stream);
+  hipMemsetAsync(ws, 0, zero_bytes, stream);
   hist_edges<<<512, 256, 0, stream>>>(ei, cnt);
   scan2x<<<2, 256, 0, stream>>>(cnt, rowptr, cur);
   scatter_edges<<<512, 256, 0, stream>>>(ei, cur, col_s, perm_s, col_d, perm_d);
 
-  gemm512<<<256, 256, 0, stream>>>(x, p1w1, gcn1_w, xw1, h1);
+  int omA = NS(), omB = NS();
+
+  gemm512k<<<dim3(256, 2), 256, 0, stream>>>(x, p1w1, gcn1_w, xw1, h1);
   edge_gate1<<<2048, 256, 0, stream>>>(xw1, ei, p1b1, p1w2, p1b2,
-                                       out + 131073, deg1, SC + 0);
-  gather_w2<<<512, 256, 0, stream>>>(out + 131073, perm_s, perm_d, w1s, w1d);
-  make_dis<<<16, 256, 0, stream>>>(deg1, dis1);
-  spmm<64, 1><<<1024, 256, 0, stream>>>(rp_d, col_d, w1d, h1, dis1, P, SC, -1, 0.f, -1, -1);
-  conv_epi64<<<1024, 256, 0, stream>>>(P, h1, dis1, gcn1_b, x1);
+                                       out + 131073, deg1, SC);
+  gatherdis_om<<<512, 256, 0, stream>>>(out + 131073, perm_s, perm_d, w1s, w1d,
+                                        deg1, dis1, omega1, omega2, SC, omA, omB);
+  conv1f<<<1024, 256, 0, stream>>>(rp_d, col_d, w1d, h1, dis1, gcn1_b, x1);
 
   gemm64<<<128, 256, 0, stream>>>(x1, p2w1, gcn2_w, x1w, h2);
   edge_gate2<<<1024, 256, 0, stream>>>(x1w, ei, p2b1, p2w2, p2b2,
                                        out + 262145, deg2, SC + 2);
-  gather_w2<<<512, 256, 0, stream>>>(out + 262145, perm_s, perm_d, w2s, w2d);
-  make_dis<<<16, 256, 0, stream>>>(deg2, dis2);
-  spmm<16, 1><<<1024, 256, 0, stream>>>(rp_d, col_d, w2d, h2, dis2, P2, SC, -1, 0.f, -1, -1);
-  conv2_softmax<<<16, 256, 0, stream>>>(P2, h2, dis2, gcn2_b, out, out + 65536, SC);
-
-  {
-    int s0a = NS(), s0b = NS();
-    pad8c2<<<16, 256, 0, stream>>>(omega1, OmA, omega2, OmB, SC, s0a, s0b);
-    spmm2<8, 8><<<1024, 256, 0, stream>>>(rp_s, col_s, w1s, w2s, OmA, OmB, QA, QB,
-                                          SC, s0a, s0b, GEPS, -1, -1, -1, -1);
-    int g0a = NG(), g0b = NG();
-    gram2<<<16, 256, 0, stream>>>(QA, QB, Gd + g0a, Gd + g0b);
-    int cqa = NS(), cqb = NS();
-    chol2<<<16, 256, 0, stream>>>(QA, Gd + g0a, cqa, QB, Gd + g0b, cqb, SC);
-    for (int itp = 0; itp < 2; ++itp) {
-      spmm2<8, 8><<<1024, 256, 0, stream>>>(rp_d, col_d, w1d, w2d, QA, QB, ZA, ZB,
-                                            SC, cqa, cqb, GEPS, -1, -1, -1, -1);
-      int gza = NG(), gzb = NG();
-      gram2<<<16, 256, 0, stream>>>(ZA, ZB, Gd + gza, Gd + gzb);
-      int cza = NS(), czb = NS();
-      chol2<<<16, 256, 0, stream>>>(ZA, Gd + gza, cza, ZB, Gd + gzb, czb, SC);
-      spmm2<8, 8><<<1024, 256, 0, stream>>>(rp_s, col_s, w1s, w2s, ZA, ZB, QA, QB,
-                                            SC, cza, czb, GEPS, -1, -1, -1, -1);
-      int gqa = NG(), gqb = NG();
-      gram2<<<16, 256, 0, stream>>>(QA, QB, Gd + gqa, Gd + gqb);
-      cqa = NS(); cqb = NS();
-      chol2<<<16, 256, 0, stream>>>(QA, Gd + gqa, cqa, QB, Gd + gqb, cqb, SC);
-    }
-    spmm2<8, 8><<<1024, 256, 0, stream>>>(rp_d, col_d, w1d, w2d, QA, QB, BtA, BtB,
-                                          SC, cqa, cqb, GEPS, -1, -1, -1, -1);
-    int gba = NG(), gbb = NG();
-    gram2<<<16, 256, 0, stream>>>(BtA, BtB, Gd + gba, Gd + gbb);
-    jacobi2<<<1, 128, 0, stream>>>(Gd + gba, Gd + gbb, SMFA, SMFB);
-    v_scale2<<<16, 256, 0, stream>>>(BtA, SMFA, BtB, SMFB, V8A, V8B);
-  }
-
-  int nyB0;
-  {
-    int sWa = NS(), sWb = NS();
-    pack3c2<<<16, 256, 0, stream>>>(V8A, WA, V8B, WB, SC, sWa, sWb);
-    int sTa = NS(), sTb = NS();
-    spmm2<4, 4><<<1024, 256, 0, stream>>>(rp_d, col_d, w1d, w2d, WA, WB, TA, TB,
-                                          SC, sWa, sWb, GEPS, sTa, -1, sTb, -1);
-    int sYa = NS(), sYb = NS(), nyA = NS(), nyB = NS();
-    spmm2<4, 4><<<1024, 256, 0, stream>>>(rp_s, col_s, w1s, w2s, TA, TB, YA, YB,
-                                          SC, sTa, sTb, GEPS, sYa, nyA, sYb, nyB);
-    int zzA = NS(), zzB = NS();
-    spmm2<4, 4><<<1024, 256, 0, stream>>>(rp_d, col_d, w1d, w2d, YA, YB, ZZA, ZZB,
-                                          SC, sYa, sYb, GEPS, -1, zzA, -1, zzB);
-    accum2b<<<1, 1, 0, stream>>>(SC, zzA, nyA, zzB, nyB);
-    vscale2<<<16, 256, 0, stream>>>(UvA, YA, 4, 2, nyA + 2,
-                                    UvB, YB, 4, 2, nyB + 2, SC);
-    nyB0 = nyB;
-  }
-
-  {
-    int sWp = NS();
-    build_Wc<<<16, 256, 0, stream>>>(WB, 4, 1, 0, ZZB, 4, 2, nullptr, SC, nyB0 + 2, SC, sWp);
-    spmm<4, 0><<<1024, 256, 0, stream>>>(rp_s, col_s, w2s, WB, nullptr, P4, SC, sWp, GEPS, -1, -1);
-    vscale1<<<16, 256, 0, stream>>>(Pv, P4, 4, 0, SC, -1);
-  }
+  gatherdis_om<<<512, 256, 0, stream>>>(out + 262145, perm_s, perm_d, w2s, w2d,
+                                        deg2, dis2, nullptr, nullptr, SC, 0, 0);
+  conv2f<<<1024, 256, 0, stream>>>(rp_d, col_d, w2d, h2, dis2, gcn2_b, xo);
+  softmax_calib<<<16, 256, 0, stream>>>(xo, out, out + 65536, SC);
+
+  int g0a = NG(), g0b = NG(), g1a = NG(), g1b = NG(), g2a = NG(), g2b = NG();
+  int g3a = NG(), g3b = NG(), g4a = NG(), g4b = NG(), g5a = NG(), g5b = NG();
+  int c0a = NS(), c0b = NS(), c1a = NS(), c1b = NS(), c2a = NS(), c2b = NS();
+  int c3a = NS(), c3b = NS(), c4a = NS(), c4b = NS(), c5a = NS(), c5b = NS();
+  spmm8f<0, 6><<<512, 256, 0, stream>>>(rp_s, col_s, w1s, w2s, omega1, omega2,
+                                        QA, QB, nullptr, nullptr, Gd + g0a, Gd + g0b,
+                                        SC, omA, omB, c0a, c0b);
+  spmm8f<1, 8><<<512, 256, 0, stream>>>(rp_d, col_d, w1d, w2d, QA, QB, ZA, ZB,
+                                        Gd + g0a, Gd + g0b, Gd + g1a, Gd + g1b,
+                                        SC, c0a, c0b, c1a, c1b);
+  spmm8f<1, 8><<<512, 256, 0, stream>>>(rp_s, col_s, w1s, w2s, ZA, ZB, QA, QB,
+                                        Gd + g1a, Gd + g1b, Gd + g2a, Gd + g2b,
+                                        SC, c1a, c1b, c2a, c2b);
+  spmm8f<1, 8><<<512, 256, 0, stream>>>(rp_d, col_d, w1d, w2d, QA, QB, ZA, ZB,
+                                        Gd + g2a, Gd + g2b, Gd + g3a, Gd + g3b,
+                                        SC, c2a, c2b, c3a, c3b);
+  spmm8f<1, 8><<<512, 256, 0, stream>>>(rp_s, col_s, w1s, w2s, ZA, ZB, QA, QB,
+                                        Gd + g3a, Gd + g3b, Gd + g4a, Gd + g4b,
+                                        SC, c3a, c3b, c4a, c4b);
+  spmm8f<1, 8><<<512, 256, 0, stream>>>(rp_d, col_d, w1d, w2d, QA, QB, BtA, BtB,
+                                        Gd + g4a, Gd + g4b, Gd + g5a, Gd + g5b,
+                                        SC, c4a, c4b, c5a, c5b);
+  jacobi2<<<1, 128, 0, stream>>>(Gd + g5a, Gd + g5b, SMFA, SMFB);
+  v_scale2<<<16, 256, 0, stream>>>(BtA, SMFA, BtB, SMFB, V8A, V8B);
+
+  int sWa = NS(), sWb = NS();
+  pack3c2<<<16, 256, 0, stream>>>(V8A, WA, V8B, WB, SC, sWa, sWb);
+  int sTa = NS(), sTb = NS();
+  spmm2<4, 4><<<1024, 256, 0, stream>>>(rp_d, col_d, w1d, w2d, WA, WB, TA, TB,
+                                        SC, sWa, sWb, GEPS, sTa, -1, sTb, -1);
+  int sYa = NS(), sYb = NS(), nyA = NS(), nyB = NS();
+  spmm2<4, 4><<<1024, 256, 0, stream>>>(rp_s, col_s, w1s, w2s, TA, TB, YA, YB,
+                                        SC, sTa, sTb, GEPS, sYa, nyA, sYb, nyB);
+  int zzA = NS(), zzB = NS();
+  spmm2<4, 4><<<1024, 256, 0, stream>>>(rp_d, col_d, w1d, w2d, YA, YB, ZZA, ZZB,
+                                        SC, sYa, sYb, GEPS, -1, zzA, -1, zzB);
+  int sWp = NS();
+  b3post<<<16, 256, 0, stream>>>(YA, YB, ZZB, UvA, UvB, WB, SC, zzA, nyA, zzB, nyB, sWp);
+  spmm<4, 0><<<1024, 256, 0, stream>>>(rp_s, col_s, w2s, WB, nullptr, P4, SC, sWp,
+                                       GEPS, -1, -1);
 
   for (int k = 3; k <= 5; ++k) {
     const int nu = k - 2, nt = 1 << nu, nd = k - 2;
     const int FA = (k < 5) ? 4 : 8;
-    int sWa = NS(), sWb = NS(), C = NS(), sTa = NS(), sTb = NS();
-    int nyA2 = NS(), nyB2 = NS(), sW2a = NS(), sW2b = NS(), zzA2 = NS(), zzB2 = NS(), dp = NS();
-    buildAB<<<32, 256, 0, stream>>>(WA, FA, nt, nu, V8A, k, UvA, SC, sWa,
-                                    WB, V8B, UvB, nd, sWb, C);
+    int dWa = NS(), dWb = NS(), C = NS();
+    int dTa = NS(), dTb = NS();
+    int nyA2 = NS(), nyB2 = NS(), sW2a = NS(), sW2b = NS(), zzA2 = NS(), zzB2 = NS();
+    int dp = NS(), sW3 = NS();
+    buildAB<<<32, 256, 0, stream>>>(WA, FA, nt, nu, V8A, k, UvA, SC, dWa,
+                                    WB, V8B, UvB, nd, dWb, C, P4, Pv, (k == 3) ? 1 : 0);
     if (FA == 4) {
       spmm2<4, 4><<<1024, 256, 0, stream>>>(rp_d, col_d, w1d, w2d, WA, WB, TA, TB,
-                                            SC, sWa, sWb, GEPS, sTa, -1, sTb, -1);
+                                            SC, dWa, dWb, GEPS, dTa, -1, dTb, -1);
       spmm2<4, 4><<<1024, 256, 0, stream>>>(rp_s, col_s, w1s, w2s, TA, TB, YA, YB,
-                                            SC, sTa, sTb, GEPS, -1, -1, -1, -1);
+                                            SC, dTa, dTb, GEPS, -1, -1, -1, -1);
     } else {
       spmm2<8, 4><<<1024, 256, 0, stream>>>(rp_d, col_d, w1d, w2d, WA, WB, TA, TB,
-                                            SC, sWa, sWb, GEPS, sTa, -1, sTb, -1);
+                                            SC, dWa, dWb, GEPS, dTa, -1, dTb, -1);
       spmm2<8, 4><<<1024, 256, 0, stream>>>(rp_s, col_s, w1s, w2s, TA, TB, YA, YB,
-                                            SC, sTa, sTb, GEPS, -1, -1, -1, -1);
+                                            SC, dTa, dTb, GEPS, -1, -1, -1, -1);
     }
     epiAB<<<32, 256, 0, stream>>>(YA, FA, nt, nu, UvA, yvA, nyA2,
                                   YB, Pv, UvB, nd, yvB, C, nyB2, dp, SC);
-    buildAB2<<<32, 256, 0, stream>>>(WA, FA, nt, nu, yvA, UvA, sW2a,
-                                     WB, yvB, sW2b, SC);
+    buildAB2<<<32, 256, 0, stream>>>(WA, FA, nt, nu, yvA, UvA, sW2a, WB, yvB, sW2b, SC);
     if (FA == 4)
       spmm2<4, 4><<<1024, 256, 0, stream>>>(rp_d, col_d, w1d, w2d, WA, WB, ZZA, ZZB,
                                             SC, sW2a, sW2b, GEPS, -1, zzA2, -1, zzB2);
     else
       spmm2<8, 4><<<1024, 256, 0, stream>>>(rp_d, col_d, w1d, w2d, WA, WB, ZZA, ZZB,
                                             SC, sW2a, sW2b, GEPS, -1, zzA2, -1, zzB2);
-    accum2k<<<1, 1, 0, stream>>>(SC, zzA2, nt, nyA2, zzB2, nyB2, dp, nd);
     if (k < 5) {
-      vscale2<<<16, 256, 0, stream>>>(UvA + (size_t)(k - 2) * N, yvA, 1, 0, nyA2,
-                                      UvB + (size_t)(k - 2) * N, yvB, 1, 0, nyB2, SC);
-      int sW3 = NS();
-      build_Wc<<<16, 256, 0, stream>>>(WB, 4, 1, 0, ZZB, 4, 0, nullptr, SC, nyB2, SC, sW3);
-      spmm<4, 0><<<1024, 256, 0, stream>>>(rp_s, col_s, w2s, WB, nullptr, P4, SC, sW3, GEPS, -1, -1);
+      defpost<<<16, 256, 0, stream>>>(SC, zzA2, nt, nyA2, zzB2, nyB2, dp, nd,
+                                      yvA, yvB, UvA, UvB, k, ZZB, WB, sW3, 1);
+      spmm<4, 0><<<1024, 256, 0, stream>>>(rp_s, col_s, w2s, WB, nullptr, P4, SC, sW3,
+                                           GEPS, -1, -1);
       axpy_sq<<<16, 256, 0, stream>>>(Pv + (size_t)(k - 2) * N, P4, 4, 0,
                                       Pv, Pv + N, Pv + 2 * N,
                                       SC, dp + 1, dp + 3, dp + 5, nd, nyB2, -1, -1);
+    } else {
+      defpost<<<1, 256, 0, stream>>>(SC, zzA2, nt, nyA2, zzB2, nyB2, dp, nd,
+                                     yvA, yvB, UvA, UvB, k, ZZB, WB, sW3, 0);
     }
   }
 
```

New measurement: 884.9 us. 2.5% more time.
